# Optimization experiments

Measured on AMD Instinct MI355X. Metric: run time of the kernel, lower is better.

Reference implementation:

```python
import jax, jax.numpy as jnp
import numpy as np

N = 6144          # active voxels / points
C = 96            # embed_channels
B = 2             # batch size
D = H = W = 32    # sparse spatial shape
K = 16            # PFAS kNN
DEPTH = 4
GRID_OPTS = np.array([[0.1, 0.1, 0.1], [0.4, 0.4, 0.4], [0.2, 0.2, 0.2]], dtype=np.float32)
BN_EPS = 1e-5


def _bn(x, g, b):
    # BatchNorm1d in training mode: batch stats over the point dim, biased var
    m = x.mean(0)
    v = jnp.var(x, axis=0)
    return (x - m) * jax.lax.rsqrt(v + BN_EPS) * g + b


def _seg_sum(x, seg):
    return jax.ops.segment_sum(x, seg, num_segments=N)


def _forward(indices, x, fp_w, fp_b, fp_g, fp_be, att_w1, att_b1, att_w2, att_b2,
             ff_w1, ff_b1, ff_g, ff_be, ff_w2, ff_b2, sa_w1, sa_b1, sa_w2, sa_b2,
             fj_w1, fj_b1, fj_g, fj_be, fj_w2, fj_b2,
             proj_w, proj_g, proj_be, lw_w, lw_g, lw_be, w_w, adp_w,
             fuse_w, fuse_g, fuse_be, conv1_w, bn1_g, bn1_be, conv2_w, bn2_g, bn2_be):
    # ---- CMPFE ----
    p = jax.nn.relu(_bn(x @ fp_w.T + fp_b, fp_g, fp_be))            # [N,9]
    cd, cl, nm = p[:, :3], p[:, 3:6], p[:, 6:9]

    def _att(f, i):
        h = jax.nn.relu(f @ att_w1[i].T + att_b1[i])
        return jax.nn.sigmoid(h @ att_w2[i].T + att_b2[i])

    enh = jnp.concatenate([cd, cl * _att(cl, 0), nm * _att(nm, 1)], axis=1)
    fu = jax.nn.relu(_bn(enh @ ff_w1.T + ff_b1, ff_g, ff_be)) @ ff_w2.T + ff_b2
    sem = jax.nn.sigmoid(jax.nn.relu(fu @ sa_w1.T + sa_b1) @ sa_w2.T + sa_b2)
    feat = fu * sem + x * (1.0 - sem)                               # new x.features

    # ---- PFAS: kNN geometry stats ----
    coord = indices[:, 1:].astype(jnp.float32)                      # [N,3]
    batch = indices[:, 0]
    sq = jnp.sum(coord * coord, axis=1)
    d2 = sq[:, None] + sq[None, :] - 2.0 * (coord @ coord.T)
    dist = jnp.sqrt(jnp.maximum(d2, 1e-12))
    same = batch[None, :] == batch[:, None]
    eye = jnp.eye(N, dtype=bool)
    dist = jnp.where(same & ~eye, dist, jnp.inf)
    neg_nd, idx = jax.lax.top_k(-dist, K)                           # K nearest
    nbr = coord[idx]                                                # [N,K,3]
    cent = nbr - nbr.mean(axis=1, keepdims=True)
    cov = jnp.einsum('nkd,nke->nde', cent, cent) / (K - 1)
    S = jnp.linalg.svd(cov, compute_uv=False)                       # [N,3] descending
    Sn = S / (S.sum(axis=1, keepdims=True) + 1e-6)
    linearity = Sn[:, 0:1] - (Sn[:, 1] + Sn[:, 2])[:, None]
    mean_dist = (-neg_nd).mean(axis=1, keepdims=True)
    density = 1.0 / (mean_dist + 1e-6)
    fl = jax.nn.relu(_bn(feat @ fj_w1.T + fj_b1, fj_g, fj_be)) @ fj_w2.T + fj_b2
    fp_ = jax.nn.softmax(fl, axis=1)
    tower = (density * 2.0 + fp_[:, 0:1]) / 3.0
    backg = (jnp.maximum(1.0 - linearity, 1.0 - density) + fp_[:, 1:2]) / 3.0
    line = (linearity * 2.0 + fp_[:, 2:3]) / 3.0
    go = jnp.asarray(GRID_OPTS)
    lg = go[2] * jnp.array([1.0, 1.0, 5.0], jnp.float32)            # last dim *5
    grid_sizes = tower * go[0] + backg * go[1] + line * lg + 1e-6   # [N,3]

    # ---- representative grids (N > 200 path) ----
    gm = grid_sizes.mean(axis=1)
    order = jnp.argsort(gm)
    reps = [grid_sizes[order[100:200]].mean(0),
            grid_sizes[order[::-1][:100]].mean(0),
            grid_sizes[order[:100]].mean(0)]

    # ---- voxel-grid clustering (torch_geometric voxel_grid + unique inverse) ----
    start = coord.min(axis=0)

    def _cluster(size):
        size = jnp.clip(size, 1e-6, None)
        c = jnp.clip(jnp.floor((coord - start) / size).astype(jnp.int64), 0, 4095)
        mx = c.max(axis=0) + 1
        ids = ((batch.astype(jnp.int64) * mx[0] + c[:, 0]) * mx[1] + c[:, 1]) * mx[2] + c[:, 2]
        _, inv = jnp.unique(ids, return_inverse=True, size=N, fill_value=0)
        return inv.reshape(-1)

    # ---- adaptive multi-branch scatter softmax aggregation ----
    branch_feats = []
    for i in range(DEPTH - 1):
        seg = _cluster(reps[i])
        cnt = jnp.maximum(_seg_sum(jnp.ones((N, 1), feat.dtype), seg), 1.0)
        pw = jax.nn.relu(_bn(feat @ lw_w[i].T, lw_g[i], lw_be[i]))
        pw = pw - (_seg_sum(pw, seg) / cnt)[seg]
        pw = pw @ w_w[i].T
        pw = jnp.exp(pw - pw.max())
        pw = pw / (_seg_sum(pw, seg)[seg] + 1e-6)
        pf = jax.nn.relu(_bn(feat @ proj_w[i].T, proj_g[i], proj_be[i])) * pw
        branch_feats.append(_seg_sum(pf, seg)[seg])
    adp = jax.nn.softmax(feat @ adp_w.T, axis=1)                    # [N,3]
    agg = jnp.einsum('nc,ncd->nd', adp, jnp.stack(branch_feats, 1))
    last = jax.nn.relu(_bn(feat @ proj_w[-1].T, proj_g[-1], proj_be[-1]))
    fused = jax.nn.relu(_bn(jnp.concatenate([last, agg], 1) @ fuse_w.T, fuse_g, fuse_be)) + feat
    res = fused

    # ---- submanifold sparse conv block (dense scatter form; inactive sites zero,
    #      outputs gathered only at active sites == SubMConv3d) ----
    bi, zi, yi, xi = indices[:, 0], indices[:, 1], indices[:, 2], indices[:, 3]

    def _subm(f, w):
        grid = jnp.zeros((B, D, H, W, C), f.dtype).at[bi, zi, yi, xi].set(f)
        o = jax.lax.conv_general_dilated(grid, w, (1, 1, 1), 'SAME',
                                         dimension_numbers=('NDHWC', 'DHWIO', 'NDHWC'))
        return o[bi, zi, yi, xi]

    f1 = jax.nn.relu(_bn(_subm(fused, conv1_w), bn1_g, bn1_be))
    f2 = _bn(_subm(f1, conv2_w), bn2_g, bn2_be)
    return jax.nn.relu(f2 + res)


def setup_inputs() -> dict:
    key = jax.random.key(0)
    ks = iter(jax.random.split(key, 64))

    def rn(*shape, s=0.05):
        return jax.random.normal(next(ks), shape, jnp.float32) * s

    # unique active voxel coordinates
    rng = np.random.default_rng(0)
    flat = rng.choice(B * D * H * W, size=N, replace=False)
    b = flat // (D * H * W)
    r = flat % (D * H * W)
    z = r // (H * W)
    y = (r % (H * W)) // W
    xw = r % W
    indices = jnp.asarray(np.stack([b, z, y, xw], 1).astype(np.int32))
    Ch = C // 2
    return {
        'x': jax.random.normal(next(ks), (N, C), jnp.float32),
        'indices': indices,
        'fp_w': rn(9, C), 'fp_b': rn(9), 'fp_g': jnp.ones(9), 'fp_be': jnp.zeros(9),
        'att_w1': rn(2, 16, 3), 'att_b1': rn(2, 16), 'att_w2': rn(2, 3, 16), 'att_b2': rn(2, 3),
        'ff_w1': rn(C, 9), 'ff_b1': rn(C), 'ff_g': jnp.ones(C), 'ff_be': jnp.zeros(C),
        'ff_w2': rn(C, C), 'ff_b2': rn(C),
        'sa_w1': rn(Ch, C), 'sa_b1': rn(Ch), 'sa_w2': rn(1, Ch), 'sa_b2': rn(1),
        'fj_w1': rn(64, C), 'fj_b1': rn(64), 'fj_g': jnp.ones(64), 'fj_be': jnp.zeros(64),
        'fj_w2': rn(3, 64), 'fj_b2': rn(3),
        'proj_w': rn(DEPTH, C, C), 'proj_g': jnp.ones((DEPTH, C)), 'proj_be': jnp.zeros((DEPTH, C)),
        'lw_w': rn(DEPTH - 1, C, C), 'lw_g': jnp.ones((DEPTH - 1, C)), 'lw_be': jnp.zeros((DEPTH - 1, C)),
        'w_w': rn(DEPTH - 1, C, C),
        'adp_w': rn(DEPTH - 1, C),
        'fuse_w': rn(C, 2 * C), 'fuse_g': jnp.ones(C), 'fuse_be': jnp.zeros(C),
        'conv1_w': rn(3, 3, 3, C, C), 'bn1_g': jnp.ones(C), 'bn1_be': jnp.zeros(C),
        'conv2_w': rn(3, 3, 3, C, C), 'bn2_g': jnp.ones(C), 'bn2_be': jnp.zeros(C),
    }


def reference(x, indices, fp_w, fp_b, fp_g, fp_be, att_w1, att_b1, att_w2, att_b2,
              ff_w1, ff_b1, ff_g, ff_be, ff_w2, ff_b2, sa_w1, sa_b1, sa_w2, sa_b2,
              fj_w1, fj_b1, fj_g, fj_be, fj_w2, fj_b2,
              proj_w, proj_g, proj_be, lw_w, lw_g, lw_be, w_w, adp_w,
              fuse_w, fuse_g, fuse_be, conv1_w, bn1_g, bn1_be, conv2_w, bn2_g, bn2_be):
    return _forward(indices, x, fp_w, fp_b, fp_g, fp_be, att_w1, att_b1, att_w2, att_b2,
                    ff_w1, ff_b1, ff_g, ff_be, ff_w2, ff_b2, sa_w1, sa_b1, sa_w2, sa_b2,
                    fj_w1, fj_b1, fj_g, fj_be, fj_w2, fj_b2,
                    proj_w, proj_g, proj_be, lw_w, lw_g, lw_be, w_w, adp_w,
                    fuse_w, fuse_g, fuse_be, conv1_w, bn1_g, bn1_be, conv2_w, bn2_g, bn2_be)
```

## Files before the change

kernel.cpp:

```cpp
#include <hip/hip_runtime.h>
#include <cstdint>

#define NPTS 6144
#define CH 96
#define NCELEM (NPTS*CH)
#define HTSZ 16384
#define NBALL 514

__device__ __forceinline__ unsigned fenc(float f){
  unsigned u = __float_as_uint(f);
  return (u & 0x80000000u) ? ~u : (u | 0x80000000u);
}
__device__ __forceinline__ float fdec(unsigned u){
  unsigned b = (u & 0x80000000u) ? (u & 0x7FFFFFFFu) : ~u;
  return __uint_as_float(b);
}

__device__ void eig3(double a00,double a01,double a02,double a11,double a12,double a22,
                     double &e0,double &e1,double &e2){
  double p1 = a01*a01 + a02*a02 + a12*a12;
  double q = (a00+a11+a22)/3.0;
  double b00=a00-q, b11=a11-q, b22=a22-q;
  double p2 = b00*b00 + b11*b11 + b22*b22 + 2.0*p1;
  if (p2 <= 1e-300){ e0=e1=e2=q; return; }
  double pp = sqrt(p2/6.0);
  double inv = 1.0/pp;
  double c00=b00*inv, c01=a01*inv, c02=a02*inv, c11=b11*inv, c12=a12*inv, c22=b22*inv;
  double det = c00*(c11*c22-c12*c12) - c01*(c01*c22-c12*c02) + c02*(c01*c12-c11*c02);
  double r = det*0.5;
  r = r < -1.0 ? -1.0 : (r > 1.0 ? 1.0 : r);
  double phi = acos(r)/3.0;
  e0 = q + 2.0*pp*cos(phi);
  e2 = q + 2.0*pp*cos(phi + 2.0943951023931953);
  e1 = 3.0*q - e0 - e2;
}

__global__ void k_zero(int* p, long n){
  long i = (long)blockIdx.x*blockDim.x + threadIdx.x;
  long st = (long)gridDim.x*blockDim.x;
  for (; i < n; i += st) p[i] = 0;
}
__global__ void k_init(int* table, int* startmin){
  int i = blockIdx.x*blockDim.x + threadIdx.x;
  if (i < 2*32*32*32) table[i] = -1;
  if (i < 3) startmin[i] = 0x7fffffff;
}
__global__ void k_htinit(unsigned long long* keys, int* vals){
  int i = blockIdx.x*blockDim.x + threadIdx.x;
  if (i < 3*HTSZ){ keys[i] = ~0ull; vals[i] = 0x7fffffff; }
}
__global__ void k_pack_min(const int* __restrict__ ind, unsigned* __restrict__ packed, int* startmin){
  __shared__ int mn[3];
  if (threadIdx.x < 3) mn[threadIdx.x] = 0x7fffffff;
  __syncthreads();
  int p = blockIdx.x*blockDim.x + threadIdx.x;
  if (p < NPTS){
    int b = ind[p*4], z = ind[p*4+1], y = ind[p*4+2], x = ind[p*4+3];
    packed[p] = (unsigned)((b<<15)|(z<<10)|(y<<5)|x);
    atomicMin(&mn[0], z); atomicMin(&mn[1], y); atomicMin(&mn[2], x);
  }
  __syncthreads();
  if (threadIdx.x < 3) atomicMin(&startmin[threadIdx.x], mn[threadIdx.x]);
}
__global__ void k_ball(unsigned* __restrict__ ball){
  __shared__ int hcnt[32], hbase[32], hpos[32];
  int tid = threadIdx.x;
  if (tid < 32){ hcnt[tid] = 0; hpos[tid] = 0; }
  __syncthreads();
  for (int i=tid; i<1331; i+=256){
    int dz = i/121, rm = i - dz*121, dy = rm/11, dx = rm - dy*11;
    int a = dz-5, b = dy-5, c = dx-5;
    int d2 = a*a + b*b + c*c;
    if (d2 > 0 && d2 <= 25) atomicAdd(&hcnt[d2], 1);
  }
  __syncthreads();
  if (tid == 0){
    int acc = 0;
    for (int d=1; d<=25; ++d){ hbase[d] = acc; acc += hcnt[d]; }
  }
  __syncthreads();
  for (int i=tid; i<1331; i+=256){
    int dz = i/121, rm = i - dz*121, dy = rm/11, dx = rm - dy*11;
    int a = dz-5, b = dy-5, c = dx-5;
    int d2 = a*a + b*b + c*c;
    if (d2 > 0 && d2 <= 25){
      int pos = hbase[d2] + atomicAdd(&hpos[d2], 1);
      ball[pos] = ((unsigned)d2<<16)|((unsigned)dz<<10)|((unsigned)dy<<5)|(unsigned)dx;
    }
  }
}

__global__ void __launch_bounds__(256) k_mm(
    const float* __restrict__ Abase, const float* __restrict__ Wbase,
    const float* __restrict__ biasBase, float* __restrict__ Obase,
    int CIN, int COUT,
    long sA, long sW, long sO, long sBias,
    const float* __restrict__ statsBase, long sStats,
    const float* __restrict__ gBase, const float* __restrict__ beBase, long sGB,
    const float* __restrict__ SsumBase, const int* __restrict__ segBase, const int* __restrict__ cntBase,
    unsigned* maxenc, int mode)
{
  int zb = blockIdx.y;
  const float* A = Abase + (long)zb*sA;
  const float* W = Wbase + (long)zb*sW;
  float* O = Obase + (long)zb*sO;
  const float* st = statsBase ? statsBase + (long)zb*sStats : nullptr;
  const float* g  = gBase ? gBase + (long)zb*sGB : nullptr;
  const float* be = beBase ? beBase + (long)zb*sGB : nullptr;
  const float* Ss = SsumBase ? SsumBase + (long)zb*NCELEM : nullptr;
  const int* seg  = segBase ? segBase + (long)zb*NPTS : nullptr;
  const int* cnt  = cntBase ? cntBase + (long)zb*NPTS : nullptr;

  __shared__ float Alt[96*34];
  __shared__ float Wlt[96*98];
  int tid = threadIdx.x;
  int r0 = blockIdx.x*32;
  for (int idx = tid; idx < CIN*COUT; idx += 256){
    int co = idx / CIN, k = idx - co*CIN;
    Wlt[k*98 + co] = W[idx];
  }
  for (int idx = tid; idx < 32*CIN; idx += 256){
    int ir = idx / CIN, k = idx - ir*CIN;
    int row = r0 + ir;
    float v = A[(long)row*CIN + k];
    if (mode >= 1) v = fmaxf((v - st[k*2])*st[k*2+1]*g[k] + be[k], 0.f);
    if (mode == 2){
      int s = seg[row];
      float cf = fmaxf((float)cnt[s], 1.f);
      v -= Ss[(long)s*CH + k] / cf;
    }
    Alt[k*34 + ir] = v;
  }
  __syncthreads();
  float lmax = -3.4e38f;
  if (COUT == 96){
    int rp = tid >> 4, cg = tid & 15;
    int co0 = cg*6;
    float acc0[6], acc1[6];
    #pragma unroll
    for (int j=0;j<6;++j){
      float b = biasBase ? biasBase[(long)zb*sBias + co0 + j] : 0.f;
      acc0[j] = b; acc1[j] = b;
    }
    int ra = 2*rp;
    for (int k=0;k<CIN;++k){
      float2 a  = *(const float2*)&Alt[k*34 + ra];
      float2 w0 = *(const float2*)&Wlt[k*98 + co0];
      float2 w1 = *(const float2*)&Wlt[k*98 + co0 + 2];
      float2 w2 = *(const float2*)&Wlt[k*98 + co0 + 4];
      acc0[0] = fmaf(a.x, w0.x, acc0[0]); acc1[0] = fmaf(a.y, w0.x, acc1[0]);
      acc0[1] = fmaf(a.x, w0.y, acc0[1]); acc1[1] = fmaf(a.y, w0.y, acc1[1]);
      acc0[2] = fmaf(a.x, w1.x, acc0[2]); acc1[2] = fmaf(a.y, w1.x, acc1[2]);
      acc0[3] = fmaf(a.x, w1.y, acc0[3]); acc1[3] = fmaf(a.y, w1.y, acc1[3]);
      acc0[4] = fmaf(a.x, w2.x, acc0[4]); acc1[4] = fmaf(a.y, w2.x, acc1[4]);
      acc0[5] = fmaf(a.x, w2.y, acc0[5]); acc1[5] = fmaf(a.y, w2.y, acc1[5]);
    }
    int rb = ra+1;
    #pragma unroll
    for (int j=0;j<6;++j){
      O[(long)(r0+ra)*96 + co0 + j] = acc0[j];
      O[(long)(r0+rb)*96 + co0 + j] = acc1[j];
      lmax = fmaxf(lmax, fmaxf(acc0[j], acc1[j]));
    }
  } else {
    for (int idx = tid; idx < 32*COUT; idx += 256){
      int ir = idx/COUT, co = idx - ir*COUT;
      float acc = biasBase ? biasBase[(long)zb*sBias + co] : 0.f;
      for (int k=0;k<CIN;++k) acc = fmaf(Alt[k*34+ir], Wlt[k*98+co], acc);
      O[(long)(r0+ir)*COUT + co] = acc;
      lmax = fmaxf(lmax, acc);
    }
  }
  if (maxenc){
    __shared__ float rmx[256];
    rmx[tid] = lmax; __syncthreads();
    for (int s2=128; s2>0; s2>>=1){
      if (tid < s2) rmx[tid] = fmaxf(rmx[tid], rmx[tid+s2]);
      __syncthreads();
    }
    if (tid == 0) atomicMax(&maxenc[zb], fenc(rmx[0]));
  }
}

__global__ void __launch_bounds__(256) k_mm_fuse(
    const float* __restrict__ tp3, const float* __restrict__ st,
    const float* __restrict__ pg3, const float* __restrict__ pbe3,
    const float* __restrict__ agg, const float* __restrict__ fw, float* __restrict__ tf)
{
  __shared__ float Alt[192*34];
  __shared__ float Wlt[96*98];
  int tid = threadIdx.x, r0 = blockIdx.x*32;
  for (int idx = tid; idx < 32*192; idx += 256){
    int ir = idx/192, k = idx - ir*192;
    int row = r0 + ir;
    float v;
    if (k < 96){
      v = tp3[(long)row*96 + k];
      v = fmaxf((v - st[k*2])*st[k*2+1]*pg3[k] + pbe3[k], 0.f);
    } else {
      v = agg[(long)row*96 + (k-96)];
    }
    Alt[k*34 + ir] = v;
  }
  int rp = tid >> 4, cg = tid & 15, co0 = cg*6;
  float acc0[6] = {0,0,0,0,0,0}, acc1[6] = {0,0,0,0,0,0};
  int ra = 2*rp, rb = ra+1;
  for (int h=0; h<2; ++h){
    __syncthreads();
    for (int idx = tid; idx < 96*96; idx += 256){
      int co = idx/96, k = idx - co*96;
      Wlt[k*98+co] = fw[(long)co*192 + h*96 + k];
    }
    __syncthreads();
    for (int k=0;k<96;++k){
      float2 a  = *(const float2*)&Alt[(h*96 + k)*34 + ra];
      float2 w0 = *(const float2*)&Wlt[k*98 + co0];
      float2 w1 = *(const float2*)&Wlt[k*98 + co0 + 2];
      float2 w2 = *(const float2*)&Wlt[k*98 + co0 + 4];
      acc0[0] = fmaf(a.x, w0.x, acc0[0]); acc1[0] = fmaf(a.y, w0.x, acc1[0]);
      acc0[1] = fmaf(a.x, w0.y, acc0[1]); acc1[1] = fmaf(a.y, w0.y, acc1[1]);
      acc0[2] = fmaf(a.x, w1.x, acc0[2]); acc1[2] = fmaf(a.y, w1.x, acc1[2]);
      acc0[3] = fmaf(a.x, w1.y, acc0[3]); acc1[3] = fmaf(a.y, w1.y, acc1[3]);
      acc0[4] = fmaf(a.x, w2.x, acc0[4]); acc1[4] = fmaf(a.y, w2.x, acc1[4]);
      acc0[5] = fmaf(a.x, w2.y, acc0[5]); acc1[5] = fmaf(a.y, w2.y, acc1[5]);
    }
  }
  #pragma unroll
  for (int j=0;j<6;++j){
    tf[(long)(r0+ra)*96 + co0 + j] = acc0[j];
    tf[(long)(r0+rb)*96 + co0 + j] = acc1[j];
  }
}

__global__ void k_stats(const float* __restrict__ Abase, long sA, int COLS,
                        float* __restrict__ statsBase, long sStats){
  int col = blockIdx.x, zb = blockIdx.y;
  const float* A = Abase + (long)zb*sA;
  double s = 0.0, q = 0.0;
  for (int r = threadIdx.x; r < NPTS; r += 256){
    double v = (double)A[(long)r*COLS + col];
    s += v; q += v*v;
  }
  __shared__ double ls[256], lq[256];
  ls[threadIdx.x] = s; lq[threadIdx.x] = q; __syncthreads();
  for (int t=128; t>0; t>>=1){
    if (threadIdx.x < t){ ls[threadIdx.x] += ls[threadIdx.x+t]; lq[threadIdx.x] += lq[threadIdx.x+t]; }
    __syncthreads();
  }
  if (threadIdx.x == 0){
    double mean = ls[0]/NPTS;
    double var = lq[0]/NPTS - mean*mean;
    float* stp = statsBase + (long)zb*sStats + col*2;
    stp[0] = (float)mean;
    stp[1] = (float)(1.0/sqrt(var + 1e-5));
  }
}

__global__ void k_p_att_enh(const float* __restrict__ t9, const float* __restrict__ st,
                            const float* __restrict__ fg, const float* __restrict__ fbe,
                            const float* __restrict__ aw1, const float* __restrict__ ab1,
                            const float* __restrict__ aw2, const float* __restrict__ ab2,
                            float* __restrict__ enh){
  int p = blockIdx.x*blockDim.x + threadIdx.x;
  if (p >= NPTS) return;
  float pp[9];
  #pragma unroll
  for (int c=0;c<9;++c){
    float v = t9[p*9+c];
    pp[c] = fmaxf((v - st[c*2])*st[c*2+1]*fg[c] + fbe[c], 0.f);
  }
  float eo[9];
  eo[0]=pp[0]; eo[1]=pp[1]; eo[2]=pp[2];
  #pragma unroll
  for (int i=0;i<2;++i){
    const float* w1 = aw1 + i*48;
    const float* b1 = ab1 + i*16;
    const float* w2 = aw2 + i*48;
    const float* b2 = ab2 + i*3;
    const float* f = pp + 3 + i*3;
    float h[16];
    #pragma unroll
    for (int j=0;j<16;++j){
      float s = b1[j];
      #pragma unroll
      for (int k=0;k<3;++k) s = fmaf(f[k], w1[j*3+k], s);
      h[j] = fmaxf(s, 0.f);
    }
    #pragma unroll
    for (int o=0;o<3;++o){
      float s = b2[o];
      #pragma unroll
      for (int j=0;j<16;++j) s = fmaf(h[j], w2[o*16+j], s);
      float a = 1.f/(1.f + expf(-s));
      eo[3+i*3+o] = f[o]*a;
    }
  }
  #pragma unroll
  for (int c=0;c<9;++c) enh[p*9+c] = eo[c];
}

__global__ void __launch_bounds__(256) k_sem_feat(
    const float* __restrict__ fu, const float* __restrict__ x,
    const float* __restrict__ w1, const float* __restrict__ b1,
    const float* __restrict__ w2, const float* __restrict__ b2,
    float* __restrict__ feat){
  int wid = (blockIdx.x*blockDim.x + threadIdx.x) >> 6;
  int lane = threadIdx.x & 63;
  if (wid >= NPTS) return;
  const float* fr = fu + (long)wid*96;
  float partial = 0.f;
  if (lane < 48){
    float h = b1[lane];
    for (int k=0;k<96;++k) h = fmaf(fr[k], w1[lane*96+k], h);
    h = fmaxf(h, 0.f);
    partial = h * w2[lane];
  }
  for (int m=32; m; m>>=1) partial += __shfl_xor(partial, m);
  float sem = 1.f/(1.f + expf(-(partial + b2[0])));
  for (int c=lane; c<96; c+=64){
    float f = fr[c];
    feat[(long)wid*96+c] = f*sem + x[(long)wid*96+c]*(1.f - sem);
  }
}

__global__ void __launch_bounds__(256) k_knn(const unsigned* __restrict__ packed,
                                             const int* __restrict__ table,
                                             const unsigned* __restrict__ ball,
                                             float* __restrict__ density, float* __restrict__ linearity){
  __shared__ unsigned pk[NPTS];
  for (int i=threadIdx.x; i<NPTS; i+=256) pk[i] = packed[i];
  __syncthreads();
  int pid = blockIdx.x*4 + (threadIdx.x>>6);
  int lane = threadIdx.x & 63;
  unsigned mypc = pk[pid];
  int myb = (int)(mypc>>15);
  int mz = (int)((mypc>>10)&31), my_=(int)((mypc>>5)&31), mx_=(int)(mypc&31);
  unsigned s[16];
  #pragma unroll
  for (int t=0;t<16;++t) s[t] = 0xFFFFFFFFu;
  int cnt = 0;
  const int tbase = myb*32768;
  for (int it=0; it<9; ++it){
    int i = lane + it*64;
    if (i < NBALL){
      unsigned e = ball[i];
      int d2 = (int)(e >> 16);
      int dz = (int)((e>>10)&31) - 5;
      int dy = (int)((e>>5)&31) - 5;
      int dx = (int)(e&31) - 5;
      int zz = mz+dz, yy = my_+dy, xx = mx_+dx;
      if ((unsigned)zz < 32u && (unsigned)yy < 32u && (unsigned)xx < 32u){
        int j = table[tbase + (zz*32+yy)*32+xx];
        if (j >= 0){
          ++cnt;
          unsigned key = ((unsigned)d2<<13) | (unsigned)j;
          if (key < s[15]){
            s[15] = key;
            #pragma unroll
            for (int t=15;t>0;--t){
              unsigned a = s[t-1], b = s[t];
              unsigned lo = a<b?a:b, hi = a<b?b:a;
              s[t-1]=lo; s[t]=hi;
            }
          }
        }
      }
    }
    int nxt = (it+1)*64;
    if (nxt >= NBALL) break;
    int tot = cnt;
    for (int m=32; m; m>>=1) tot += __shfl_xor(tot, m);
    unsigned dlast = ball[nxt-1] >> 16;
    unsigned dnext = ball[nxt] >> 16;
    if (tot >= 16 && dnext > dlast) break;
  }
  int tot = cnt;
  for (int m=32; m; m>>=1) tot += __shfl_xor(tot, m);
  if (tot < 16){
    #pragma unroll
    for (int t=0;t<16;++t) s[t] = 0xFFFFFFFFu;
    for (int it=0; it<96; ++it){
      int j = lane + it*64;
      unsigned pc = pk[j];
      if (j != pid && (int)(pc>>15) == myb){
        int dz = (int)((pc>>10)&31) - mz;
        int dy = (int)((pc>>5)&31) - my_;
        int dx = (int)(pc&31) - mx_;
        unsigned d2 = (unsigned)(dz*dz + dy*dy + dx*dx);
        unsigned key = (d2<<13) | (unsigned)j;
        if (key < s[15]){
          s[15] = key;
          #pragma unroll
          for (int t=15;t>0;--t){
            unsigned a = s[t-1], b = s[t];
            unsigned lo = a<b?a:b, hi = a<b?b:a;
            s[t-1]=lo; s[t]=hi;
          }
        }
      }
    }
  }
  float sdist = 0.f;
  int sz=0,sy=0,sx=0,szz=0,syy=0,sxx=0,szy=0,szx=0,syx=0;
  for (int r=0;r<16;++r){
    unsigned m = s[0];
    #pragma unroll
    for (int w=32; w; w>>=1){
      unsigned o = (unsigned)__shfl_xor((int)m, w);
      m = m<o ? m : o;
    }
    bool own = (s[0] == m);
    #pragma unroll
    for (int t=0;t<15;++t) s[t] = own ? s[t+1] : s[t];
    if (own) s[15] = 0xFFFFFFFFu;
    unsigned idx = m & 8191u;
    unsigned d2 = m >> 13;
    sdist += sqrtf((float)d2);
    unsigned pc = pk[idx];
    int nz=(int)((pc>>10)&31), ny=(int)((pc>>5)&31), nx=(int)(pc&31);
    sz+=nz; sy+=ny; sx+=nx;
    szz+=nz*nz; syy+=ny*ny; sxx+=nx*nx; szy+=nz*ny; szx+=nz*nx; syx+=ny*nx;
  }
  if (lane == 0){
    double m0 = sz/16.0, m1 = sy/16.0, m2 = sx/16.0;
    float c00 = (float)(((double)szz - 16.0*m0*m0)/15.0);
    float c11 = (float)(((double)syy - 16.0*m1*m1)/15.0);
    float c22 = (float)(((double)sxx - 16.0*m2*m2)/15.0);
    float c01 = (float)(((double)szy - 16.0*m0*m1)/15.0);
    float c02 = (float)(((double)szx - 16.0*m0*m2)/15.0);
    float c12 = (float)(((double)syx - 16.0*m1*m2)/15.0);
    double e0,e1,e2;
    eig3((double)c00,(double)c01,(double)c02,(double)c11,(double)c12,(double)c22, e0,e1,e2);
    float s0 = (float)fabs(e0), s1 = (float)fabs(e1), s2 = (float)fabs(e2);
    float den = s0 + s1 + s2 + 1e-6f;
    float sn0 = s0/den, sn1 = s1/den, sn2 = s2/den;
    linearity[pid] = sn0 - (sn1 + sn2);
    float md = sdist * (1.f/16.f);
    density[pid] = 1.f/(md + 1e-6f);
  }
}

__global__ void k_geo(const float* __restrict__ t64, const float* __restrict__ st,
                      const float* __restrict__ fg, const float* __restrict__ fbe,
                      const float* __restrict__ w2, const float* __restrict__ b2,
                      const float* __restrict__ density, const float* __restrict__ linearity,
                      float* __restrict__ gsz, float* __restrict__ gm){
  int p = blockIdx.x*blockDim.x + threadIdx.x;
  if (p >= NPTS) return;
  float fl[3];
  #pragma unroll
  for (int o=0;o<3;++o) fl[o] = b2[o];
  for (int k=0;k<64;++k){
    float v = t64[(long)p*64+k];
    v = fmaxf((v - st[k*2])*st[k*2+1]*fg[k] + fbe[k], 0.f);
    #pragma unroll
    for (int o=0;o<3;++o) fl[o] = fmaf(v, w2[o*64+k], fl[o]);
  }
  float mx = fmaxf(fl[0], fmaxf(fl[1], fl[2]));
  float e0 = expf(fl[0]-mx), e1 = expf(fl[1]-mx), e2 = expf(fl[2]-mx);
  float es = e0+e1+e2;
  float p0 = e0/es, p1 = e1/es, p2 = e2/es;
  float den = density[p], lin = linearity[p];
  float tw = (den*2.f + p0)/3.f;
  float bg = (fmaxf(1.f-lin, 1.f-den) + p1)/3.f;
  float ln = (lin*2.f + p2)/3.f;
  float g0 = tw*0.1f + bg*0.4f + ln*0.2f + 1e-6f;
  float g1 = tw*0.1f + bg*0.4f + ln*0.2f + 1e-6f;
  float g2 = tw*0.1f + bg*0.4f + ln*1.0f + 1e-6f;
  gsz[p*3+0]=g0; gsz[p*3+1]=g1; gsz[p*3+2]=g2;
  gm[p] = (g0+g1+g2)/3.f;
}

#define RNKCHUNK 768
__global__ void __launch_bounds__(256) k_rank(const float* __restrict__ gm, int* __restrict__ rank){
  __shared__ unsigned long long lk[RNKCHUNK];
  int j0 = blockIdx.y*RNKCHUNK;
  for (int i=threadIdx.x; i<RNKCHUNK; i+=256){
    int j = j0 + i;
    lk[i] = (((unsigned long long)fenc(gm[j]))<<13) | (unsigned long long)j;
  }
  __syncthreads();
  int p = blockIdx.x*256 + threadIdx.x;
  unsigned long long myk = (((unsigned long long)fenc(gm[p]))<<13) | (unsigned long long)p;
  int cnt = 0;
  #pragma unroll 4
  for (int i=0; i<RNKCHUNK; ++i) cnt += (lk[i] < myk) ? 1 : 0;
  atomicAdd(&rank[p], cnt);
}
__global__ void k_scatter(const int* __restrict__ rank, const float* __restrict__ gsz,
                          float* __restrict__ bkt){
  int p = blockIdx.x*blockDim.x + threadIdx.x;
  if (p >= NPTS) return;
  int r = rank[p];
  int z = -1, t = 0;
  if (r < 100){ z = 2; t = r; }
  else if (r < 200){ z = 0; t = r - 100; }
  else if (r >= NPTS-100){ z = 1; t = r - (NPTS-100); }
  if (z >= 0){
    #pragma unroll
    for (int d=0; d<3; ++d) bkt[(z*100 + t)*3 + d] = gsz[p*3+d];
  }
}
__global__ void k_reps(const float* __restrict__ bkt, float* __restrict__ reps){
  int i = threadIdx.x;
  if (i >= 9) return;
  int z = i/3, d = i - z*3;
  double s = 0.0;
  for (int t=0; t<100; ++t) s += (double)bkt[(z*100 + t)*3 + d];
  reps[i] = (float)(s/100.0);
}

__global__ void k_cluster_c(const int* __restrict__ ind, const float* __restrict__ reps,
                            const int* __restrict__ startmin, int* __restrict__ cbuf, int* mxbuf){
  int z = blockIdx.y;
  int p = blockIdx.x*blockDim.x + threadIdx.x;
  __shared__ int lmx[3];
  if (threadIdx.x < 3) lmx[threadIdx.x] = 0;
  __syncthreads();
  if (p < NPTS){
    #pragma unroll
    for (int d=0; d<3; ++d){
      float sizev = fmaxf(reps[z*3+d], 1e-6f);
      float cf = floorf(((float)ind[p*4+1+d] - (float)startmin[d]) / sizev);
      int ci = (int)cf;
      ci = ci < 0 ? 0 : (ci > 4095 ? 4095 : ci);
      cbuf[((long)z*NPTS + p)*3 + d] = ci;
      atomicMax(&lmx[d], ci);
    }
  }
  __syncthreads();
  if (threadIdx.x < 3) atomicMax(&mxbuf[z*3+threadIdx.x], lmx[threadIdx.x]);
}
__global__ void k_cluster_ids(const int* __restrict__ ind, const int* __restrict__ cbuf,
                              const int* __restrict__ mxbuf, long long* __restrict__ ids){
  int z = blockIdx.y;
  int p = blockIdx.x*blockDim.x + threadIdx.x;
  if (p >= NPTS) return;
  long long mx0 = mxbuf[z*3+0]+1, mx1 = mxbuf[z*3+1]+1, mx2 = mxbuf[z*3+2]+1;
  long long b = ind[p*4];
  const int* cc = cbuf + ((long)z*NPTS + p)*3;
  ids[(long)z*NPTS + p] = ((b*mx0 + cc[0])*mx1 + cc[1])*mx2 + cc[2];
}

__device__ __forceinline__ int ht_hash(unsigned long long id){
  unsigned long long h = id * 0x9E3779B97F4A7C15ull;
  return (int)(h >> 49) & (HTSZ-1);
}
__global__ void k_seg_build(const long long* __restrict__ ids,
                            unsigned long long* __restrict__ keys, int* __restrict__ vals){
  int z = blockIdx.y;
  int p = blockIdx.x*blockDim.x + threadIdx.x;
  if (p >= NPTS) return;
  unsigned long long id = (unsigned long long)ids[(long)z*NPTS + p];
  unsigned long long* K = keys + (long)z*HTSZ;
  int* V = vals + (long)z*HTSZ;
  int slot = ht_hash(id);
  while (true){
    unsigned long long prev = atomicCAS(&K[slot], ~0ull, id);
    if (prev == ~0ull || prev == id){ atomicMin(&V[slot], p); break; }
    slot = (slot + 1) & (HTSZ-1);
  }
}
__global__ void k_seg_lookup(const long long* __restrict__ ids,
                             const unsigned long long* __restrict__ keys, const int* __restrict__ vals,
                             int* __restrict__ seg, int* __restrict__ cnt){
  int z = blockIdx.y;
  int p = blockIdx.x*blockDim.x + threadIdx.x;
  if (p >= NPTS) return;
  unsigned long long id = (unsigned long long)ids[(long)z*NPTS + p];
  const unsigned long long* K = keys + (long)z*HTSZ;
  int slot = ht_hash(id);
  while (K[slot] != id) slot = (slot + 1) & (HTSZ-1);
  int rep = vals[(long)z*HTSZ + slot];
  seg[(long)z*NPTS + p] = rep;
  atomicAdd(&cnt[(long)z*NPTS + rep], 1);
}

__global__ void k_pw_accum(const float* __restrict__ tlw, const float* __restrict__ stats,
                           const float* __restrict__ g, const float* __restrict__ be,
                           const int* __restrict__ seg, float* __restrict__ S){
  int z = blockIdx.y;
  int idx = blockIdx.x*blockDim.x + threadIdx.x;
  int p = idx/CH, c = idx - p*CH;
  const float* st = stats + z*192;
  float v = tlw[(long)z*NCELEM + idx];
  v = fmaxf((v - st[c*2])*st[c*2+1]*g[z*CH+c] + be[z*CH+c], 0.f);
  atomicAdd(&S[(long)z*NCELEM + (long)seg[(long)z*NPTS+p]*CH + c], v);
}
__global__ void k_exp_accum(const float* __restrict__ pw2, const unsigned* __restrict__ maxenc,
                            const int* __restrict__ seg, float* __restrict__ E){
  int z = blockIdx.y;
  int idx = blockIdx.x*blockDim.x + threadIdx.x;
  int p = idx/CH, c = idx - p*CH;
  float mv = fdec(maxenc[z]);
  float v = expf(pw2[(long)z*NCELEM + idx] - mv);
  atomicAdd(&E[(long)z*NCELEM + (long)seg[(long)z*NPTS+p]*CH + c], v);
}
__global__ void k_pf_accum(const float* __restrict__ tp, const float* __restrict__ stats,
                           const float* __restrict__ pg, const float* __restrict__ pbe,
                           const float* __restrict__ pw2, const unsigned* __restrict__ maxenc,
                           const int* __restrict__ seg, const float* __restrict__ E,
                           float* __restrict__ F){
  int z = blockIdx.y;
  int idx = blockIdx.x*blockDim.x + threadIdx.x;
  int p = idx/CH, c = idx - p*CH;
  const float* st = stats + z*192;
  float v = tp[(long)z*NCELEM + idx];
  v = fmaxf((v - st[c*2])*st[c*2+1]*pg[z*CH+c] + pbe[z*CH+c], 0.f);
  float mv = fdec(maxenc[z]);
  int sg = seg[(long)z*NPTS+p];
  float w = expf(pw2[(long)z*NCELEM + idx] - mv) / (E[(long)z*NCELEM + (long)sg*CH + c] + 1e-6f);
  atomicAdd(&F[(long)z*NCELEM + (long)sg*CH + c], v*w);
}
__global__ void k_adp(const float* __restrict__ feat, const float* __restrict__ aw,
                      float* __restrict__ adp){
  int p = blockIdx.x*blockDim.x + threadIdx.x;
  if (p >= NPTS) return;
  float a0=0.f, a1=0.f, a2=0.f;
  for (int k=0;k<CH;++k){
    float f = feat[(long)p*CH+k];
    a0 = fmaf(f, aw[k], a0);
    a1 = fmaf(f, aw[CH+k], a1);
    a2 = fmaf(f, aw[2*CH+k], a2);
  }
  float m = fmaxf(a0, fmaxf(a1,a2));
  float e0 = expf(a0-m), e1 = expf(a1-m), e2 = expf(a2-m);
  float s = e0+e1+e2;
  adp[p*3]=e0/s; adp[p*3+1]=e1/s; adp[p*3+2]=e2/s;
}
__global__ void k_agg(const float* __restrict__ adp, const float* __restrict__ F,
                      const int* __restrict__ seg, float* __restrict__ agg){
  int idx = blockIdx.x*blockDim.x + threadIdx.x;
  int p = idx/CH, c = idx - p*CH;
  float s = 0.f;
  #pragma unroll
  for (int z=0;z<3;++z)
    s = fmaf(adp[p*3+z], F[(long)z*NCELEM + (long)seg[(long)z*NPTS+p]*CH + c], s);
  agg[idx] = s;
}

__global__ void k_fused(const float* __restrict__ tf, const float* __restrict__ st,
                        const float* __restrict__ fg, const float* __restrict__ fbe,
                        const float* __restrict__ feat, float* __restrict__ fused){
  int idx = blockIdx.x*blockDim.x + threadIdx.x;
  int c = idx % CH;
  float v = tf[idx];
  v = fmaxf((v - st[c*2])*st[c*2+1]*fg[c] + fbe[c], 0.f);
  fused[idx] = v + feat[idx];
}
__global__ void k_table(const int* __restrict__ ind, int* __restrict__ table){
  int p = blockIdx.x*blockDim.x + threadIdx.x;
  if (p >= NPTS) return;
  int b = ind[p*4], z = ind[p*4+1], y = ind[p*4+2], x = ind[p*4+3];
  table[((b*32+z)*32+y)*32+x] = p;
}
__global__ void k_nbr(const int* __restrict__ ind, const int* __restrict__ table,
                      int* __restrict__ nbrtab){
  int idx = blockIdx.x*blockDim.x + threadIdx.x;
  if (idx >= NPTS*27) return;
  int p = idx/27, tap = idx - p*27;
  int dz = tap/9 - 1;
  int rm = tap % 9;
  int dy = rm/3 - 1, dx = rm%3 - 1;
  int b = ind[p*4], z = ind[p*4+1]+dz, y = ind[p*4+2]+dy, x = ind[p*4+3]+dx;
  int q = -1;
  if ((unsigned)z < 32u && (unsigned)y < 32u && (unsigned)x < 32u)
    q = table[((b*32+z)*32+y)*32+x];
  nbrtab[idx] = q;
}
__global__ void __launch_bounds__(256) k_convlist(const int* __restrict__ nbrtab,
                                                  int* __restrict__ tapcnt,
                                                  int* __restrict__ ptlist){
  __shared__ int lcnt[27], lbase[27], lpos[27];
  int tid = threadIdx.x;
  if (tid < 27){ lcnt[tid] = 0; lpos[tid] = 0; }
  __syncthreads();
  int base = blockIdx.x * 6912;
  for (int i = tid; i < 6912; i += 256){
    int idx = base + i;
    if (nbrtab[idx] >= 0) atomicAdd(&lcnt[idx % 27], 1);
  }
  __syncthreads();
  if (tid < 27) lbase[tid] = atomicAdd(&tapcnt[tid], lcnt[tid]);
  __syncthreads();
  for (int i = tid; i < 6912; i += 256){
    int idx = base + i;
    int q = nbrtab[idx];
    if (q >= 0){
      int tap = idx % 27;
      int p = idx / 27;
      int pos = lbase[tap] + atomicAdd(&lpos[tap], 1);
      ptlist[tap*NPTS + pos] = (p<<16) | q;
    }
  }
}
__global__ void __launch_bounds__(256) k_conv_gemm(
    const float* __restrict__ src, const float* __restrict__ Wc,
    const int* __restrict__ tapcnt, const int* __restrict__ ptlist,
    float* __restrict__ part){
  int tap = blockIdx.y;
  int n = tapcnt[tap];
  int r0 = blockIdx.x*32;
  if (r0 >= n) return;
  __shared__ float Alt[96*34];
  __shared__ float Wlt[96*98];
  __shared__ int pqs[32];
  int tid = threadIdx.x;
  if (tid < 32){
    int r = r0 + tid;
    pqs[tid] = (r < n) ? ptlist[tap*NPTS + r] : -1;
  }
  __syncthreads();
  for (int idx4 = tid; idx4 < 2304; idx4 += 256){
    int ci = idx4/24, c4 = idx4 - ci*24;
    float4 w = ((const float4*)(Wc + ((long)tap*96 + ci)*96))[c4];
    float* d = &Wlt[ci*98 + c4*4];
    d[0]=w.x; d[1]=w.y; d[2]=w.z; d[3]=w.w;
  }
  for (int idx4 = tid; idx4 < 32*24; idx4 += 256){
    int ir = idx4/24, c4 = idx4 - ir*24;
    int pq = pqs[ir];
    float4 s = make_float4(0.f,0.f,0.f,0.f);
    if (pq >= 0){
      int q = pq & 0xFFFF;
      s = ((const float4*)(src + (long)q*CH))[c4];
    }
    int k0 = c4*4;
    Alt[(k0+0)*34 + ir] = s.x;
    Alt[(k0+1)*34 + ir] = s.y;
    Alt[(k0+2)*34 + ir] = s.z;
    Alt[(k0+3)*34 + ir] = s.w;
  }
  __syncthreads();
  int rp = tid >> 4, cg = tid & 15;
  int co0 = cg*6;
  int ra = 2*rp, rb = ra+1;
  float acc0[6]={0,0,0,0,0,0}, acc1[6]={0,0,0,0,0,0};
  for (int k=0;k<96;++k){
    float2 a  = *(const float2*)&Alt[k*34 + ra];
    float2 w0 = *(const float2*)&Wlt[k*98 + co0];
    float2 w1 = *(const float2*)&Wlt[k*98 + co0 + 2];
    float2 w2 = *(const float2*)&Wlt[k*98 + co0 + 4];
    acc0[0] = fmaf(a.x, w0.x, acc0[0]); acc1[0] = fmaf(a.y, w0.x, acc1[0]);
    acc0[1] = fmaf(a.x, w0.y, acc0[1]); acc1[1] = fmaf(a.y, w0.y, acc1[1]);
    acc0[2] = fmaf(a.x, w1.x, acc0[2]); acc1[2] = fmaf(a.y, w1.x, acc1[2]);
    acc0[3] = fmaf(a.x, w1.y, acc0[3]); acc1[3] = fmaf(a.y, w1.y, acc1[3]);
    acc0[4] = fmaf(a.x, w2.x, acc0[4]); acc1[4] = fmaf(a.y, w2.x, acc1[4]);
    acc0[5] = fmaf(a.x, w2.y, acc0[5]); acc1[5] = fmaf(a.y, w2.y, acc1[5]);
  }
  int pa = pqs[ra], pb = pqs[rb];
  if (pa >= 0){
    float* o = part + ((long)(pa>>16)*27 + tap)*CH + co0;
    #pragma unroll
    for (int j=0;j<6;++j) o[j] = acc0[j];
  }
  if (pb >= 0){
    float* o = part + ((long)(pb>>16)*27 + tap)*CH + co0;
    #pragma unroll
    for (int j=0;j<6;++j) o[j] = acc1[j];
  }
}
__global__ void __launch_bounds__(256) k_conv_sum(const int* __restrict__ nbrtab,
                                                  const float* __restrict__ part,
                                                  float* __restrict__ out){
  int idx = blockIdx.x*256 + threadIdx.x;
  int p = idx/24, c4 = idx - p*24;
  const int* nt = nbrtab + p*27;
  float4 acc = make_float4(0.f,0.f,0.f,0.f);
  for (int tap=0; tap<27; ++tap){
    if (nt[tap] >= 0){
      float4 v = ((const float4*)part)[((long)p*27 + tap)*24 + c4];
      acc.x += v.x; acc.y += v.y; acc.z += v.z; acc.w += v.w;
    }
  }
  ((float4*)out)[idx] = acc;
}
__global__ void __launch_bounds__(256) k_conv_gemm_atomic(
    const float* __restrict__ src, const float* __restrict__ Wc,
    const int* __restrict__ tapcnt, const int* __restrict__ ptlist,
    float* __restrict__ out){
  int tap = blockIdx.y;
  int n = tapcnt[tap];
  int r0 = blockIdx.x*32;
  if (r0 >= n) return;
  __shared__ float Al[32*97];
  __shared__ float Wl[96*97];
  __shared__ int pqs[32];
  int tid = threadIdx.x;
  if (tid < 32){
    int r = r0 + tid;
    pqs[tid] = (r < n) ? ptlist[tap*NPTS + r] : -1;
  }
  __syncthreads();
  for (int idx4 = tid; idx4 < 2304; idx4 += 256){
    int ci = idx4/24, c4 = idx4 - ci*24;
    float4 w = ((const float4*)(Wc + ((long)tap*96 + ci)*96))[c4];
    float* d = &Wl[ci*97 + c4*4];
    d[0]=w.x; d[1]=w.y; d[2]=w.z; d[3]=w.w;
  }
  for (int idx4 = tid; idx4 < 32*24; idx4 += 256){
    int ir = idx4/24, c4 = idx4 - ir*24;
    int pq = pqs[ir];
    float4 s = make_float4(0.f,0.f,0.f,0.f);
    if (pq >= 0){
      int q = pq & 0xFFFF;
      s = ((const float4*)(src + (long)q*CH))[c4];
    }
    float* d = &Al[ir*97 + c4*4];
    d[0]=s.x; d[1]=s.y; d[2]=s.z; d[3]=s.w;
  }
  __syncthreads();
  int rp = tid >> 4, cg = tid & 15;
  int co0 = cg*6;
  int ra = 2*rp, rb = ra+1;
  float acc0[6]={0,0,0,0,0,0}, acc1[6]={0,0,0,0,0,0};
  for (int k=0;k<96;++k){
    float a0 = Al[ra*97+k], a1 = Al[rb*97+k];
    #pragma unroll
    for (int j=0;j<6;++j){
      float w = Wl[k*97+co0+j];
      acc0[j] = fmaf(a0, w, acc0[j]);
      acc1[j] = fmaf(a1, w, acc1[j]);
    }
  }
  int pa = pqs[ra], pb = pqs[rb];
  if (pa >= 0){
    float* o = out + (long)(pa>>16)*CH + co0;
    #pragma unroll
    for (int j=0;j<6;++j) atomicAdd(&o[j], acc0[j]);
  }
  if (pb >= 0){
    float* o = out + (long)(pb>>16)*CH + co0;
    #pragma unroll
    for (int j=0;j<6;++j) atomicAdd(&o[j], acc1[j]);
  }
}
__global__ void k_bnrelu(const float* __restrict__ a, const float* __restrict__ st,
                         const float* __restrict__ g, const float* __restrict__ be,
                         float* __restrict__ o){
  int idx = blockIdx.x*blockDim.x + threadIdx.x;
  int c = idx % CH;
  float v = a[idx];
  o[idx] = fmaxf((v - st[c*2])*st[c*2+1]*g[c] + be[c], 0.f);
}
__global__ void k_final(const float* __restrict__ c2, const float* __restrict__ st,
                        const float* __restrict__ g, const float* __restrict__ be,
                        const float* __restrict__ fused, float* __restrict__ out){
  int idx = blockIdx.x*blockDim.x + threadIdx.x;
  int c = idx % CH;
  float v = c2[idx];
  v = (v - st[c*2])*st[c*2+1]*g[c] + be[c];
  out[idx] = fmaxf(v + fused[idx], 0.f);
}

extern "C" void kernel_launch(void* const* d_in, const int* in_sizes, int n_in,
                              void* d_out, int out_size, void* d_ws, size_t ws_size,
                              hipStream_t stream)
{
  const float* x      = (const float*)d_in[0];
  const int*   ind    = (const int*)  d_in[1];
  const float* fp_w   = (const float*)d_in[2];
  const float* fp_b   = (const float*)d_in[3];
  const float* fp_g   = (const float*)d_in[4];
  const float* fp_be  = (const float*)d_in[5];
  const float* att_w1 = (const float*)d_in[6];
  const float* att_b1 = (const float*)d_in[7];
  const float* att_w2 = (const float*)d_in[8];
  const float* att_b2 = (const float*)d_in[9];
  const float* ff_w1  = (const float*)d_in[10];
  const float* ff_b1  = (const float*)d_in[11];
  const float* ff_g   = (const float*)d_in[12];
  const float* ff_be  = (const float*)d_in[13];
  const float* ff_w2  = (const float*)d_in[14];
  const float* ff_b2  = (const float*)d_in[15];
  const float* sa_w1  = (const float*)d_in[16];
  const float* sa_b1  = (const float*)d_in[17];
  const float* sa_w2  = (const float*)d_in[18];
  const float* sa_b2  = (const float*)d_in[19];
  const float* fj_w1  = (const float*)d_in[20];
  const float* fj_b1  = (const float*)d_in[21];
  const float* fj_g   = (const float*)d_in[22];
  const float* fj_be  = (const float*)d_in[23];
  const float* fj_w2  = (const float*)d_in[24];
  const float* fj_b2  = (const float*)d_in[25];
  const float* proj_w = (const float*)d_in[26];
  const float* proj_g = (const float*)d_in[27];
  const float* proj_be= (const float*)d_in[28];
  const float* lw_w   = (const float*)d_in[29];
  const float* lw_g   = (const float*)d_in[30];
  const float* lw_be  = (const float*)d_in[31];
  const float* w_w    = (const float*)d_in[32];
  const float* adp_w  = (const float*)d_in[33];
  const float* fuse_w = (const float*)d_in[34];
  const float* fuse_g = (const float*)d_in[35];
  const float* fuse_be= (const float*)d_in[36];
  const float* conv1_w= (const float*)d_in[37];
  const float* bn1_g  = (const float*)d_in[38];
  const float* bn1_be = (const float*)d_in[39];
  const float* conv2_w= (const float*)d_in[40];
  const float* bn2_g  = (const float*)d_in[41];
  const float* bn2_be = (const float*)d_in[42];
  float* outp = (float*)d_out;
  (void)in_sizes; (void)n_in; (void)out_size;

  char* ws = (char*)d_ws;
  size_t off = 0;
  auto alloc = [&](size_t bytes)->size_t{
    off = (off + 255) & ~(size_t)255;
    size_t o = off; off += bytes; return o;
  };
  const size_t FNC = (size_t)NCELEM*4;
  size_t o_packed = alloc((size_t)NPTS*4);
  size_t o_start  = alloc(16);
  size_t o_ball   = alloc((size_t)NBALL*4);
  size_t o_dens   = alloc((size_t)NPTS*4);
  size_t o_lin    = alloc((size_t)NPTS*4);
  size_t o_t9     = alloc((size_t)NPTS*9*4);
  size_t o_enh    = alloc((size_t)NPTS*9*4);
  size_t o_gm     = alloc((size_t)NPTS*4);
  size_t o_gsz    = alloc((size_t)NPTS*3*4);
  size_t o_reps   = alloc(16*4);
  size_t o_bkt    = alloc((size_t)3*100*3*4);
  size_t o_cbuf   = alloc((size_t)3*NPTS*3*4);
  size_t o_ids    = alloc((size_t)3*NPTS*8);
  size_t o_seg    = alloc((size_t)3*NPTS*4);
  size_t o_adp    = alloc((size_t)NPTS*3*4);
  size_t o_table  = alloc((size_t)65536*4);
  size_t o_nbr    = alloc((size_t)NPTS*27*4);
  size_t o_ptlist = alloc((size_t)27*NPTS*4);
  size_t o_t64    = alloc((size_t)NPTS*64*4);
  size_t o_stats  = alloc((size_t)13*192*4);
  size_t o_htk    = alloc((size_t)3*HTSZ*8);
  size_t o_htv    = alloc((size_t)3*HTSZ*4);
  size_t o_S      = alloc(3*FNC);
  size_t o_E      = alloc(3*FNC);
  size_t o_F      = alloc(3*FNC);
  size_t o_cnt    = alloc((size_t)3*NPTS*4);
  size_t o_rank   = alloc((size_t)NPTS*4);
  size_t o_tapcnt = alloc(32*4);
  size_t o_mx     = alloc(16*4);
  size_t o_maxenc = alloc(16*4);
  size_t zend = off;
  size_t o_T96 = alloc(FNC);
  size_t o_fu  = alloc(FNC);
  size_t o_feat= alloc(FNC);
  size_t o_tlw = alloc(3*FNC);
  size_t o_pw2 = alloc(3*FNC);
  size_t o_tp  = alloc(4*FNC);
  size_t o_agg = alloc(FNC);
  size_t o_tf  = alloc(FNC);
  size_t o_fsd = alloc(FNC);
  size_t o_c1  = alloc(FNC);
  size_t o_f1  = alloc(FNC);
  size_t o_c2  = alloc(FNC);
  size_t o_part = alloc((size_t)NPTS*27*CH*4);
  bool use_part = (off <= ws_size);

  float* stats = (float*)(ws + o_stats);
  long zcount = (long)((zend - o_S)/4);

  k_zero<<<dim3(2048), dim3(256), 0, stream>>>((int*)(ws+o_S), zcount);
  k_init<<<dim3(256), dim3(256), 0, stream>>>((int*)(ws+o_table), (int*)(ws+o_start));
  k_htinit<<<dim3((3*HTSZ+255)/256), dim3(256), 0, stream>>>((unsigned long long*)(ws+o_htk), (int*)(ws+o_htv));
  k_pack_min<<<dim3(24), dim3(256), 0, stream>>>(ind, (unsigned*)(ws+o_packed), (int*)(ws+o_start));
  k_table<<<dim3(24), 256, 0, stream>>>(ind, (int*)(ws+o_table));
  k_ball<<<dim3(1), 256, 0, stream>>>((unsigned*)(ws+o_ball));

  k_mm<<<dim3(192,1), 256, 0, stream>>>(x, fp_w, fp_b, (float*)(ws+o_t9), 96, 9,
      0,0,0,0, nullptr,0, nullptr,nullptr,0, nullptr,nullptr,nullptr, nullptr, 0);
  k_stats<<<dim3(9,1), 256, 0, stream>>>((float*)(ws+o_t9), 0, 9, stats+0*192, 0);
  k_p_att_enh<<<dim3(24), 256, 0, stream>>>((float*)(ws+o_t9), stats+0*192, fp_g, fp_be,
      att_w1, att_b1, att_w2, att_b2, (float*)(ws+o_enh));

  k_mm<<<dim3(192,1), 256, 0, stream>>>((float*)(ws+o_enh), ff_w1, ff_b1, (float*)(ws+o_T96), 9, 96,
      0,0,0,0, nullptr,0, nullptr,nullptr,0, nullptr,nullptr,nullptr, nullptr, 0);
  k_stats<<<dim3(96,1), 256, 0, stream>>>((float*)(ws+o_T96), 0, 96, stats+1*192, 0);
  k_mm<<<dim3(192,1), 256, 0, stream>>>((float*)(ws+o_T96), ff_w2, ff_b2, (float*)(ws+o_fu), 96, 96,
      0,0,0,0, stats+1*192,0, ff_g, ff_be,0, nullptr,nullptr,nullptr, nullptr, 1);

  k_sem_feat<<<dim3(1536), 256, 0, stream>>>((float*)(ws+o_fu), x, sa_w1, sa_b1, sa_w2, sa_b2,
      (float*)(ws+o_feat));

  k_knn<<<dim3(1536), 256, 0, stream>>>((unsigned*)(ws+o_packed), (int*)(ws+o_table),
      (unsigned*)(ws+o_ball), (float*)(ws+o_dens), (float*)(ws+o_lin));

  k_mm<<<dim3(192,1), 256, 0, stream>>>((float*)(ws+o_feat), fj_w1, fj_b1, (float*)(ws+o_t64), 96, 64,
      0,0,0,0, nullptr,0, nullptr,nullptr,0, nullptr,nullptr,nullptr, nullptr, 0);
  k_stats<<<dim3(64,1), 256, 0, stream>>>((float*)(ws+o_t64), 0, 64, stats+2*192, 0);
  k_geo<<<dim3(24), 256, 0, stream>>>((float*)(ws+o_t64), stats+2*192, fj_g, fj_be, fj_w2, fj_b2,
      (float*)(ws+o_dens), (float*)(ws+o_lin), (float*)(ws+o_gsz), (float*)(ws+o_gm));

  k_rank<<<dim3(24,8), 256, 0, stream>>>((float*)(ws+o_gm), (int*)(ws+o_rank));
  k_scatter<<<dim3(24), 256, 0, stream>>>((int*)(ws+o_rank), (float*)(ws+o_gsz), (float*)(ws+o_bkt));
  k_reps<<<dim3(1), 64, 0, stream>>>((float*)(ws+o_bkt), (float*)(ws+o_reps));

  k_cluster_c<<<dim3(24,3), 256, 0, stream>>>(ind, (float*)(ws+o_reps), (int*)(ws+o_start),
      (int*)(ws+o_cbuf), (int*)(ws+o_mx));
  k_cluster_ids<<<dim3(24,3), 256, 0, stream>>>(ind, (int*)(ws+o_cbuf), (int*)(ws+o_mx),
      (long long*)(ws+o_ids));
  k_seg_build<<<dim3(24,3), 256, 0, stream>>>((long long*)(ws+o_ids),
      (unsigned long long*)(ws+o_htk), (int*)(ws+o_htv));
  k_seg_lookup<<<dim3(24,3), 256, 0, stream>>>((long long*)(ws+o_ids),
      (unsigned long long*)(ws+o_htk), (int*)(ws+o_htv), (int*)(ws+o_seg), (int*)(ws+o_cnt));

  k_mm<<<dim3(192,3), 256, 0, stream>>>((float*)(ws+o_feat), lw_w, nullptr, (float*)(ws+o_tlw), 96, 96,
      0, 96*96, NCELEM, 0, nullptr,0, nullptr,nullptr,0, nullptr,nullptr,nullptr, nullptr, 0);
  k_stats<<<dim3(96,3), 256, 0, stream>>>((float*)(ws+o_tlw), NCELEM, 96, stats+3*192, 192);
  k_pw_accum<<<dim3(2304,3), 256, 0, stream>>>((float*)(ws+o_tlw), stats+3*192, lw_g, lw_be,
      (int*)(ws+o_seg), (float*)(ws+o_S));
  k_mm<<<dim3(192,3), 256, 0, stream>>>((float*)(ws+o_tlw), w_w, nullptr, (float*)(ws+o_pw2), 96, 96,
      NCELEM, 96*96, NCELEM, 0, stats+3*192,192, lw_g, lw_be,96,
      (float*)(ws+o_S), (int*)(ws+o_seg), (int*)(ws+o_cnt), (unsigned*)(ws+o_maxenc), 2);
  k_exp_accum<<<dim3(2304,3), 256, 0, stream>>>((float*)(ws+o_pw2), (unsigned*)(ws+o_maxenc),
      (int*)(ws+o_seg), (float*)(ws+o_E));
  k_mm<<<dim3(192,4), 256, 0, stream>>>((float*)(ws+o_feat), proj_w, nullptr, (float*)(ws+o_tp), 96, 96,
      0, 96*96, NCELEM, 0, nullptr,0, nullptr,nullptr,0, nullptr,nullptr,nullptr, nullptr, 0);
  k_stats<<<dim3(96,4), 256, 0, stream>>>((float*)(ws+o_tp), NCELEM, 96, stats+6*192, 192);
  k_pf_accum<<<dim3(2304,3), 256, 0, stream>>>((float*)(ws+o_tp), stats+6*192, proj_g, proj_be,
      (float*)(ws+o_pw2), (unsigned*)(ws+o_maxenc), (int*)(ws+o_seg), (float*)(ws+o_E), (float*)(ws+o_F));
  k_adp<<<dim3(24), 256, 0, stream>>>((float*)(ws+o_feat), adp_w, (float*)(ws+o_adp));
  k_agg<<<dim3(2304), 256, 0, stream>>>((float*)(ws+o_adp), (float*)(ws+o_F), (int*)(ws+o_seg),
      (float*)(ws+o_agg));

  k_mm_fuse<<<dim3(192), 256, 0, stream>>>((float*)(ws+o_tp) + (size_t)3*NCELEM, stats+9*192,
      proj_g + 3*96, proj_be + 3*96, (float*)(ws+o_agg), fuse_w, (float*)(ws+o_tf));
  k_stats<<<dim3(96,1), 256, 0, stream>>>((float*)(ws+o_tf), 0, 96, stats+10*192, 0);
  k_fused<<<dim3(2304), 256, 0, stream>>>((float*)(ws+o_tf), stats+10*192, fuse_g, fuse_be,
      (float*)(ws+o_feat), (float*)(ws+o_fsd));

  k_nbr<<<dim3((NPTS*27+255)/256), 256, 0, stream>>>(ind, (int*)(ws+o_table), (int*)(ws+o_nbr));
  k_convlist<<<dim3(24), 256, 0, stream>>>((int*)(ws+o_nbr), (int*)(ws+o_tapcnt),
      (int*)(ws+o_ptlist));
  if (use_part){
    k_conv_gemm<<<dim3(192,27), 256, 0, stream>>>((float*)(ws+o_fsd), conv1_w,
        (int*)(ws+o_tapcnt), (int*)(ws+o_ptlist), (float*)(ws+o_part));
    k_conv_sum<<<dim3(NPTS*24/256), 256, 0, stream>>>((int*)(ws+o_nbr), (float*)(ws+o_part),
        (float*)(ws+o_c1));
  } else {
    k_zero<<<dim3(2304), dim3(256), 0, stream>>>((int*)(ws+o_c1), NCELEM);
    k_conv_gemm_atomic<<<dim3(192,27), 256, 0, stream>>>((float*)(ws+o_fsd), conv1_w,
        (int*)(ws+o_tapcnt), (int*)(ws+o_ptlist), (float*)(ws+o_c1));
  }
  k_stats<<<dim3(96,1), 256, 0, stream>>>((float*)(ws+o_c1), 0, 96, stats+11*192, 0);
  k_bnrelu<<<dim3(2304), 256, 0, stream>>>((float*)(ws+o_c1), stats+11*192, bn1_g, bn1_be, (float*)(ws+o_f1));
  if (use_part){
    k_conv_gemm<<<dim3(192,27), 256, 0, stream>>>((float*)(ws+o_f1), conv2_w,
        (int*)(ws+o_tapcnt), (int*)(ws+o_ptlist), (float*)(ws+o_part));
    k_conv_sum<<<dim3(NPTS*24/256), 256, 0, stream>>>((int*)(ws+o_nbr), (float*)(ws+o_part),
        (float*)(ws+o_c2));
  } else {
    k_zero<<<dim3(2304), dim3(256), 0, stream>>>((int*)(ws+o_c2), NCELEM);
    k_conv_gemm_atomic<<<dim3(192,27), 256, 0, stream>>>((float*)(ws+o_f1), conv2_w,
        (int*)(ws+o_tapcnt), (int*)(ws+o_ptlist), (float*)(ws+o_c2));
  }
  k_stats<<<dim3(96,1), 256, 0, stream>>>((float*)(ws+o_c2), 0, 96, stats+12*192, 0);
  k_final<<<dim3(2304), 256, 0, stream>>>((float*)(ws+o_c2), stats+12*192, bn2_g, bn2_be,
      (float*)(ws+o_fsd), outp);
}
```

Baseline: 501.9 us.

## Fuse setup, clustering, adp/agg, and BN-ReLU into neighbouring kernels to cut launches

Merges the init kernels into one setup kernel and the pack/table/ball kernels into a second. Scatter and reps become one kernel using a last-block-done counter. The cluster max is computed from the coordinate max instead of a separate pass. k_adp and k_agg are fused, and k_nbr and k_convlist become one kernel. The fused-feature and BN1-ReLU elementwise passes are folded into the conv gather and the final kernel, removing several launches and full-tensor round trips. In exchange the BN math is recomputed per gathered neighbour in the conv load, and the derived cluster max assumes floor is monotone in the coordinate.

```diff
diff --git a/kernel.cpp b/kernel.cpp
--- a/kernel.cpp
+++ b/kernel.cpp
@@ -35,57 +35,62 @@
   e1 = 3.0*q - e0 - e2;
 }
 
-__global__ void k_zero(int* p, long n){
+__global__ void k_setup0(int* __restrict__ zb, long zcount,
+                         unsigned long long* __restrict__ htk, int* __restrict__ htv,
+                         int* __restrict__ table, int* __restrict__ startmm){
   long i = (long)blockIdx.x*blockDim.x + threadIdx.x;
   long st = (long)gridDim.x*blockDim.x;
-  for (; i < n; i += st) p[i] = 0;
-}
-__global__ void k_init(int* table, int* startmin){
-  int i = blockIdx.x*blockDim.x + threadIdx.x;
-  if (i < 2*32*32*32) table[i] = -1;
-  if (i < 3) startmin[i] = 0x7fffffff;
-}
-__global__ void k_htinit(unsigned long long* keys, int* vals){
-  int i = blockIdx.x*blockDim.x + threadIdx.x;
-  if (i < 3*HTSZ){ keys[i] = ~0ull; vals[i] = 0x7fffffff; }
-}
-__global__ void k_pack_min(const int* __restrict__ ind, unsigned* __restrict__ packed, int* startmin){
-  __shared__ int mn[3];
-  if (threadIdx.x < 3) mn[threadIdx.x] = 0x7fffffff;
-  __syncthreads();
-  int p = blockIdx.x*blockDim.x + threadIdx.x;
-  if (p < NPTS){
+  for (long j=i; j<zcount; j+=st) zb[j] = 0;
+  for (long j=i; j<3*HTSZ; j+=st){ htk[j] = ~0ull; htv[j] = 0x7fffffff; }
+  for (long j=i; j<2*32768; j+=st) table[j] = -1;
+  if (i < 3) startmm[i] = 0x7fffffff;
+  else if (i < 6) startmm[i] = 0;
+}
+__global__ void __launch_bounds__(256) k_setup1(const int* __restrict__ ind,
+                                                unsigned* __restrict__ packed,
+                                                int* __restrict__ startmm,
+                                                int* __restrict__ table,
+                                                unsigned* __restrict__ ball){
+  __shared__ int mn[3], mx[3];
+  __shared__ int hcnt[32], hbase[32], hpos[32];
+  int tid = threadIdx.x;
+  if (blockIdx.x < 24){
+    if (tid < 3){ mn[tid] = 0x7fffffff; mx[tid] = 0; }
+    __syncthreads();
+    int p = blockIdx.x*256 + tid;
     int b = ind[p*4], z = ind[p*4+1], y = ind[p*4+2], x = ind[p*4+3];
     packed[p] = (unsigned)((b<<15)|(z<<10)|(y<<5)|x);
+    table[((b*32+z)*32+y)*32+x] = p;
     atomicMin(&mn[0], z); atomicMin(&mn[1], y); atomicMin(&mn[2], x);
-  }
-  __syncthreads();
-  if (threadIdx.x < 3) atomicMin(&startmin[threadIdx.x], mn[threadIdx.x]);
-}
-__global__ void k_ball(unsigned* __restrict__ ball){
-  __shared__ int hcnt[32], hbase[32], hpos[32];
-  int tid = threadIdx.x;
-  if (tid < 32){ hcnt[tid] = 0; hpos[tid] = 0; }
-  __syncthreads();
-  for (int i=tid; i<1331; i+=256){
-    int dz = i/121, rm = i - dz*121, dy = rm/11, dx = rm - dy*11;
-    int a = dz-5, b = dy-5, c = dx-5;
-    int d2 = a*a + b*b + c*c;
-    if (d2 > 0 && d2 <= 25) atomicAdd(&hcnt[d2], 1);
-  }
-  __syncthreads();
-  if (tid == 0){
-    int acc = 0;
-    for (int d=1; d<=25; ++d){ hbase[d] = acc; acc += hcnt[d]; }
-  }
-  __syncthreads();
-  for (int i=tid; i<1331; i+=256){
-    int dz = i/121, rm = i - dz*121, dy = rm/11, dx = rm - dy*11;
-    int a = dz-5, b = dy-5, c = dx-5;
-    int d2 = a*a + b*b + c*c;
-    if (d2 > 0 && d2 <= 25){
-      int pos = hbase[d2] + atomicAdd(&hpos[d2], 1);
-      ball[pos] = ((unsigned)d2<<16)|((unsigned)dz<<10)|((unsigned)dy<<5)|(unsigned)dx;
+    atomicMax(&mx[0], z); atomicMax(&mx[1], y); atomicMax(&mx[2], x);
+    __syncthreads();
+    if (tid < 3){
+      atomicMin(&startmm[tid], mn[tid]);
+      atomicMax(&startmm[3+tid], mx[tid]);
+    }
+  } else {
+    if (tid < 32){ hcnt[tid] = 0; hpos[tid] = 0; }
+    __syncthreads();
+    for (int i=tid; i<1331; i+=256){
+      int dz = i/121, rm = i - dz*121, dy = rm/11, dx = rm - dy*11;
+      int a = dz-5, b = dy-5, c = dx-5;
+      int d2 = a*a + b*b + c*c;
+      if (d2 > 0 && d2 <= 25) atomicAdd(&hcnt[d2], 1);
+    }
+    __syncthreads();
+    if (tid == 0){
+      int acc = 0;
+      for (int d=1; d<=25; ++d){ hbase[d] = acc; acc += hcnt[d]; }
+    }
+    __syncthreads();
+    for (int i=tid; i<1331; i+=256){
+      int dz = i/121, rm = i - dz*121, dy = rm/11, dx = rm - dy*11;
+      int a = dz-5, b = dy-5, c = dx-5;
+      int d2 = a*a + b*b + c*c;
+      if (d2 > 0 && d2 <= 25){
+        int pos = hbase[d2] + atomicAdd(&hpos[d2], 1);
+        ball[pos] = ((unsigned)d2<<16)|((unsigned)dz<<10)|((unsigned)dy<<5)|(unsigned)dx;
+      }
     }
   }
 }
@@ -487,59 +492,58 @@
   for (int i=0; i<RNKCHUNK; ++i) cnt += (lk[i] < myk) ? 1 : 0;
   atomicAdd(&rank[p], cnt);
 }
-__global__ void k_scatter(const int* __restrict__ rank, const float* __restrict__ gsz,
-                          float* __restrict__ bkt){
-  int p = blockIdx.x*blockDim.x + threadIdx.x;
-  if (p >= NPTS) return;
+__global__ void __launch_bounds__(256) k_scatter_reps(const int* __restrict__ rank,
+                                                      const float* __restrict__ gsz,
+                                                      float* __restrict__ bkt,
+                                                      int* __restrict__ done,
+                                                      float* __restrict__ reps){
+  __shared__ int lastf;
+  int p = blockIdx.x*256 + threadIdx.x;
   int r = rank[p];
-  int z = -1, t = 0;
-  if (r < 100){ z = 2; t = r; }
-  else if (r < 200){ z = 0; t = r - 100; }
-  else if (r >= NPTS-100){ z = 1; t = r - (NPTS-100); }
-  if (z >= 0){
-    #pragma unroll
-    for (int d=0; d<3; ++d) bkt[(z*100 + t)*3 + d] = gsz[p*3+d];
-  }
-}
-__global__ void k_reps(const float* __restrict__ bkt, float* __restrict__ reps){
-  int i = threadIdx.x;
-  if (i >= 9) return;
-  int z = i/3, d = i - z*3;
-  double s = 0.0;
-  for (int t=0; t<100; ++t) s += (double)bkt[(z*100 + t)*3 + d];
-  reps[i] = (float)(s/100.0);
-}
-
-__global__ void k_cluster_c(const int* __restrict__ ind, const float* __restrict__ reps,
-                            const int* __restrict__ startmin, int* __restrict__ cbuf, int* mxbuf){
-  int z = blockIdx.y;
-  int p = blockIdx.x*blockDim.x + threadIdx.x;
-  __shared__ int lmx[3];
-  if (threadIdx.x < 3) lmx[threadIdx.x] = 0;
-  __syncthreads();
-  if (p < NPTS){
-    #pragma unroll
-    for (int d=0; d<3; ++d){
-      float sizev = fmaxf(reps[z*3+d], 1e-6f);
-      float cf = floorf(((float)ind[p*4+1+d] - (float)startmin[d]) / sizev);
-      int ci = (int)cf;
-      ci = ci < 0 ? 0 : (ci > 4095 ? 4095 : ci);
-      cbuf[((long)z*NPTS + p)*3 + d] = ci;
-      atomicMax(&lmx[d], ci);
-    }
-  }
-  __syncthreads();
-  if (threadIdx.x < 3) atomicMax(&mxbuf[z*3+threadIdx.x], lmx[threadIdx.x]);
-}
-__global__ void k_cluster_ids(const int* __restrict__ ind, const int* __restrict__ cbuf,
-                              const int* __restrict__ mxbuf, long long* __restrict__ ids){
+  int zb = -1, t = 0;
+  if (r < 100){ zb = 2; t = r; }
+  else if (r < 200){ zb = 0; t = r - 100; }
+  else if (r >= NPTS-100){ zb = 1; t = r - (NPTS-100); }
+  if (zb >= 0){
+    #pragma unroll
+    for (int d=0; d<3; ++d) bkt[(zb*100 + t)*3 + d] = gsz[p*3+d];
+  }
+  __threadfence();
+  __syncthreads();
+  if (threadIdx.x == 0) lastf = (atomicAdd(done, 1) == 23) ? 1 : 0;
+  __syncthreads();
+  if (lastf){
+    __threadfence();
+    int i = threadIdx.x;
+    if (i < 9){
+      int z = i/3, d = i - z*3;
+      double s = 0.0;
+      for (int tt=0; tt<100; ++tt) s += (double)bkt[(z*100 + tt)*3 + d];
+      reps[i] = (float)(s/100.0);
+    }
+  }
+}
+
+__global__ void k_cluster(const int* __restrict__ ind, const float* __restrict__ reps,
+                          const int* __restrict__ startmm, long long* __restrict__ ids){
   int z = blockIdx.y;
   int p = blockIdx.x*blockDim.x + threadIdx.x;
   if (p >= NPTS) return;
-  long long mx0 = mxbuf[z*3+0]+1, mx1 = mxbuf[z*3+1]+1, mx2 = mxbuf[z*3+2]+1;
+  long long mxp[3]; int cc[3];
+  #pragma unroll
+  for (int d=0; d<3; ++d){
+    float sizev = fmaxf(reps[z*3+d], 1e-6f);
+    float cf = floorf(((float)ind[p*4+1+d] - (float)startmm[d]) / sizev);
+    int ci = (int)cf;
+    ci = ci < 0 ? 0 : (ci > 4095 ? 4095 : ci);
+    cc[d] = ci;
+    float cfm = floorf(((float)startmm[3+d] - (float)startmm[d]) / sizev);
+    int cm = (int)cfm;
+    cm = cm < 0 ? 0 : (cm > 4095 ? 4095 : cm);
+    mxp[d] = (long long)cm + 1;
+  }
   long long b = ind[p*4];
-  const int* cc = cbuf + ((long)z*NPTS + p)*3;
-  ids[(long)z*NPTS + p] = ((b*mx0 + cc[0])*mx1 + cc[1])*mx2 + cc[2];
+  ids[(long)z*NPTS + p] = ((b*mxp[0] + cc[0])*mxp[1] + cc[1])*mxp[2] + cc[2];
 }
 
 __device__ __forceinline__ int ht_hash(unsigned long long id){
@@ -612,33 +616,46 @@
   float w = expf(pw2[(long)z*NCELEM + idx] - mv) / (E[(long)z*NCELEM + (long)sg*CH + c] + 1e-6f);
   atomicAdd(&F[(long)z*NCELEM + (long)sg*CH + c], v*w);
 }
-__global__ void k_adp(const float* __restrict__ feat, const float* __restrict__ aw,
-                      float* __restrict__ adp){
-  int p = blockIdx.x*blockDim.x + threadIdx.x;
-  if (p >= NPTS) return;
-  float a0=0.f, a1=0.f, a2=0.f;
-  for (int k=0;k<CH;++k){
-    float f = feat[(long)p*CH+k];
-    a0 = fmaf(f, aw[k], a0);
-    a1 = fmaf(f, aw[CH+k], a1);
-    a2 = fmaf(f, aw[2*CH+k], a2);
-  }
-  float m = fmaxf(a0, fmaxf(a1,a2));
-  float e0 = expf(a0-m), e1 = expf(a1-m), e2 = expf(a2-m);
-  float s = e0+e1+e2;
-  adp[p*3]=e0/s; adp[p*3+1]=e1/s; adp[p*3+2]=e2/s;
-}
-__global__ void k_agg(const float* __restrict__ adp, const float* __restrict__ F,
-                      const int* __restrict__ seg, float* __restrict__ agg){
-  int idx = blockIdx.x*blockDim.x + threadIdx.x;
-  int p = idx/CH, c = idx - p*CH;
-  float s = 0.f;
-  #pragma unroll
-  for (int z=0;z<3;++z)
-    s = fmaf(adp[p*3+z], F[(long)z*NCELEM + (long)seg[(long)z*NPTS+p]*CH + c], s);
-  agg[idx] = s;
-}
-
+__global__ void __launch_bounds__(256) k_adp_agg(
+    const float* __restrict__ feat, const float* __restrict__ aw,
+    const float* __restrict__ F, const int* __restrict__ seg,
+    float* __restrict__ agg){
+  __shared__ float ladp[32][3];
+  __shared__ int lseg[32][3];
+  int tid = threadIdx.x;
+  int p0 = blockIdx.x*32;
+  if (tid < 96){
+    int pl = tid/3, z = tid - pl*3;
+    const float* fr = feat + (long)(p0+pl)*CH;
+    float a = 0.f;
+    for (int k=0;k<CH;++k) a = fmaf(fr[k], aw[z*CH+k], a);
+    ladp[pl][z] = a;
+    lseg[pl][z] = seg[(long)z*NPTS + (p0+pl)];
+  }
+  __syncthreads();
+  if (tid < 32){
+    float a0 = ladp[tid][0], a1 = ladp[tid][1], a2 = ladp[tid][2];
+    float m = fmaxf(a0, fmaxf(a1,a2));
+    float e0 = expf(a0-m), e1 = expf(a1-m), e2 = expf(a2-m);
+    float s = e0+e1+e2;
+    ladp[tid][0]=e0/s; ladp[tid][1]=e1/s; ladp[tid][2]=e2/s;
+  }
+  __syncthreads();
+  for (int e = tid; e < 32*CH; e += 256){
+    int pl = e/CH, c = e - pl*CH;
+    float s = 0.f;
+    #pragma unroll
+    for (int z=0;z<3;++z)
+      s = fmaf(ladp[pl][z], F[(long)z*NCELEM + (long)lseg[pl][z]*CH + c], s);
+    agg[(long)p0*CH + e] = s;
+  }
+}
+
+__global__ void k_zero(int* p, long n){
+  long i = (long)blockIdx.x*blockDim.x + threadIdx.x;
+  long st = (long)gridDim.x*blockDim.x;
+  for (; i < n; i += st) p[i] = 0;
+}
 __global__ void k_fused(const float* __restrict__ tf, const float* __restrict__ st,
                         const float* __restrict__ fg, const float* __restrict__ fbe,
                         const float* __restrict__ feat, float* __restrict__ fused){
@@ -648,47 +665,57 @@
   v = fmaxf((v - st[c*2])*st[c*2+1]*fg[c] + fbe[c], 0.f);
   fused[idx] = v + feat[idx];
 }
-__global__ void k_table(const int* __restrict__ ind, int* __restrict__ table){
-  int p = blockIdx.x*blockDim.x + threadIdx.x;
-  if (p >= NPTS) return;
-  int b = ind[p*4], z = ind[p*4+1], y = ind[p*4+2], x = ind[p*4+3];
-  table[((b*32+z)*32+y)*32+x] = p;
-}
-__global__ void k_nbr(const int* __restrict__ ind, const int* __restrict__ table,
-                      int* __restrict__ nbrtab){
+__global__ void k_bnrelu(const float* __restrict__ a, const float* __restrict__ st,
+                         const float* __restrict__ g, const float* __restrict__ be,
+                         float* __restrict__ o){
   int idx = blockIdx.x*blockDim.x + threadIdx.x;
-  if (idx >= NPTS*27) return;
-  int p = idx/27, tap = idx - p*27;
-  int dz = tap/9 - 1;
-  int rm = tap % 9;
-  int dy = rm/3 - 1, dx = rm%3 - 1;
-  int b = ind[p*4], z = ind[p*4+1]+dz, y = ind[p*4+2]+dy, x = ind[p*4+3]+dx;
-  int q = -1;
-  if ((unsigned)z < 32u && (unsigned)y < 32u && (unsigned)x < 32u)
-    q = table[((b*32+z)*32+y)*32+x];
-  nbrtab[idx] = q;
-}
-__global__ void __launch_bounds__(256) k_convlist(const int* __restrict__ nbrtab,
-                                                  int* __restrict__ tapcnt,
-                                                  int* __restrict__ ptlist){
+  int c = idx % CH;
+  float v = a[idx];
+  o[idx] = fmaxf((v - st[c*2])*st[c*2+1]*g[c] + be[c], 0.f);
+}
+
+__global__ void __launch_bounds__(256) k_nbrlist(const int* __restrict__ ind,
+                                                 const int* __restrict__ table,
+                                                 int* __restrict__ nbrtab,
+                                                 int* __restrict__ tapcnt,
+                                                 int* __restrict__ ptlist){
+  __shared__ int pb[256], pz[256], py[256], px[256];
   __shared__ int lcnt[27], lbase[27], lpos[27];
   int tid = threadIdx.x;
   if (tid < 27){ lcnt[tid] = 0; lpos[tid] = 0; }
-  __syncthreads();
-  int base = blockIdx.x * 6912;
-  for (int i = tid; i < 6912; i += 256){
-    int idx = base + i;
-    if (nbrtab[idx] >= 0) atomicAdd(&lcnt[idx % 27], 1);
+  int p0 = blockIdx.x*256;
+  pb[tid] = ind[(p0+tid)*4];
+  pz[tid] = ind[(p0+tid)*4+1];
+  py[tid] = ind[(p0+tid)*4+2];
+  px[tid] = ind[(p0+tid)*4+3];
+  __syncthreads();
+  int base = blockIdx.x*6912;
+  int qv[27];
+  #pragma unroll 1
+  for (int j = 0; j < 27; ++j){
+    int i = tid + j*256;
+    int pl = i/27, tap = i - pl*27;
+    int dz = tap/9 - 1;
+    int rm = tap % 9;
+    int dy = rm/3 - 1, dx = rm%3 - 1;
+    int z = pz[pl]+dz, y = py[pl]+dy, x = px[pl]+dx;
+    int q = -1;
+    if ((unsigned)z < 32u && (unsigned)y < 32u && (unsigned)x < 32u)
+      q = table[((pb[pl]*32+z)*32+y)*32+x];
+    qv[j] = q;
+    nbrtab[base + i] = q;
+    if (q >= 0) atomicAdd(&lcnt[tap], 1);
   }
   __syncthreads();
   if (tid < 27) lbase[tid] = atomicAdd(&tapcnt[tid], lcnt[tid]);
   __syncthreads();
-  for (int i = tid; i < 6912; i += 256){
-    int idx = base + i;
-    int q = nbrtab[idx];
+  #pragma unroll 1
+  for (int j = 0; j < 27; ++j){
+    int q = qv[j];
     if (q >= 0){
-      int tap = idx % 27;
-      int p = idx / 27;
+      int i = tid + j*256;
+      int tap = i % 27;
+      int p = p0 + i/27;
       int pos = lbase[tap] + atomicAdd(&lpos[tap], 1);
       ptlist[tap*NPTS + pos] = (p<<16) | q;
     }
@@ -697,7 +724,9 @@
 __global__ void __launch_bounds__(256) k_conv_gemm(
     const float* __restrict__ src, const float* __restrict__ Wc,
     const int* __restrict__ tapcnt, const int* __restrict__ ptlist,
-    float* __restrict__ part){
+    const float* __restrict__ bnst, const float* __restrict__ bng,
+    const float* __restrict__ bnbe, const float* __restrict__ res,
+    int fmode, float* __restrict__ part){
   int tap = blockIdx.y;
   int n = tapcnt[tap];
   int r0 = blockIdx.x*32;
@@ -720,16 +749,28 @@
   for (int idx4 = tid; idx4 < 32*24; idx4 += 256){
     int ir = idx4/24, c4 = idx4 - ir*24;
     int pq = pqs[ir];
-    float4 s = make_float4(0.f,0.f,0.f,0.f);
+    float4 s4 = make_float4(0.f,0.f,0.f,0.f);
     if (pq >= 0){
       int q = pq & 0xFFFF;
-      s = ((const float4*)(src + (long)q*CH))[c4];
+      s4 = ((const float4*)(src + (long)q*CH))[c4];
+      if (fmode){
+        int c0 = c4*4;
+        float vx = fmaxf((s4.x - bnst[(c0+0)*2])*bnst[(c0+0)*2+1]*bng[c0+0] + bnbe[c0+0], 0.f);
+        float vy = fmaxf((s4.y - bnst[(c0+1)*2])*bnst[(c0+1)*2+1]*bng[c0+1] + bnbe[c0+1], 0.f);
+        float vz = fmaxf((s4.z - bnst[(c0+2)*2])*bnst[(c0+2)*2+1]*bng[c0+2] + bnbe[c0+2], 0.f);
+        float vw = fmaxf((s4.w - bnst[(c0+3)*2])*bnst[(c0+3)*2+1]*bng[c0+3] + bnbe[c0+3], 0.f);
+        if (fmode == 2){
+          const float* rr = res + (long)q*CH + c0;
+          vx += rr[0]; vy += rr[1]; vz += rr[2]; vw += rr[3];
+        }
+        s4 = make_float4(vx,vy,vz,vw);
+      }
     }
     int k0 = c4*4;
-    Alt[(k0+0)*34 + ir] = s.x;
-    Alt[(k0+1)*34 + ir] = s.y;
-    Alt[(k0+2)*34 + ir] = s.z;
-    Alt[(k0+3)*34 + ir] = s.w;
+    Alt[(k0+0)*34 + ir] = s4.x;
+    Alt[(k0+1)*34 + ir] = s4.y;
+    Alt[(k0+2)*34 + ir] = s4.z;
+    Alt[(k0+3)*34 + ir] = s4.w;
   }
   __syncthreads();
   int rp = tid >> 4, cg = tid & 15;
@@ -748,14 +789,14 @@
     acc0[4] = fmaf(a.x, w2.x, acc0[4]); acc1[4] = fmaf(a.y, w2.x, acc1[4]);
     acc0[5] = fmaf(a.x, w2.y, acc0[5]); acc1[5] = fmaf(a.y, w2.y, acc1[5]);
   }
-  int pa = pqs[ra], pb = pqs[rb];
+  int pa = pqs[ra], pb2 = pqs[rb];
   if (pa >= 0){
     float* o = part + ((long)(pa>>16)*27 + tap)*CH + co0;
     #pragma unroll
     for (int j=0;j<6;++j) o[j] = acc0[j];
   }
-  if (pb >= 0){
-    float* o = part + ((long)(pb>>16)*27 + tap)*CH + co0;
+  if (pb2 >= 0){
+    float* o = part + ((long)(pb2>>16)*27 + tap)*CH + co0;
     #pragma unroll
     for (int j=0;j<6;++j) o[j] = acc1[j];
   }
@@ -835,22 +876,16 @@
     for (int j=0;j<6;++j) atomicAdd(&o[j], acc1[j]);
   }
 }
-__global__ void k_bnrelu(const float* __restrict__ a, const float* __restrict__ st,
-                         const float* __restrict__ g, const float* __restrict__ be,
-                         float* __restrict__ o){
+__global__ void k_final(const float* __restrict__ c2, const float* __restrict__ st12,
+                        const float* __restrict__ g2, const float* __restrict__ be2,
+                        const float* __restrict__ tf, const float* __restrict__ st10,
+                        const float* __restrict__ fg, const float* __restrict__ fbe,
+                        const float* __restrict__ feat, float* __restrict__ out){
   int idx = blockIdx.x*blockDim.x + threadIdx.x;
   int c = idx % CH;
-  float v = a[idx];
-  o[idx] = fmaxf((v - st[c*2])*st[c*2+1]*g[c] + be[c], 0.f);
-}
-__global__ void k_final(const float* __restrict__ c2, const float* __restrict__ st,
-                        const float* __restrict__ g, const float* __restrict__ be,
-                        const float* __restrict__ fused, float* __restrict__ out){
-  int idx = blockIdx.x*blockDim.x + threadIdx.x;
-  int c = idx % CH;
-  float v = c2[idx];
-  v = (v - st[c*2])*st[c*2+1]*g[c] + be[c];
-  out[idx] = fmaxf(v + fused[idx], 0.f);
+  float fsd = fmaxf((tf[idx] - st10[c*2])*st10[c*2+1]*fg[c] + fbe[c], 0.f) + feat[idx];
+  float v = (c2[idx] - st12[c*2])*st12[c*2+1]*g2[c] + be2[c];
+  out[idx] = fmaxf(v + fsd, 0.f);
 }
 
 extern "C" void kernel_launch(void* const* d_in, const int* in_sizes, int n_in,
@@ -911,7 +946,7 @@
   };
   const size_t FNC = (size_t)NCELEM*4;
   size_t o_packed = alloc((size_t)NPTS*4);
-  size_t o_start  = alloc(16);
+  size_t o_start  = alloc(32);
   size_t o_ball   = alloc((size_t)NBALL*4);
   size_t o_dens   = alloc((size_t)NPTS*4);
   size_t o_lin    = alloc((size_t)NPTS*4);
@@ -921,10 +956,8 @@
   size_t o_gsz    = alloc((size_t)NPTS*3*4);
   size_t o_reps   = alloc(16*4);
   size_t o_bkt    = alloc((size_t)3*100*3*4);
-  size_t o_cbuf   = alloc((size_t)3*NPTS*3*4);
   size_t o_ids    = alloc((size_t)3*NPTS*8);
   size_t o_seg    = alloc((size_t)3*NPTS*4);
-  size_t o_adp    = alloc((size_t)NPTS*3*4);
   size_t o_table  = alloc((size_t)65536*4);
   size_t o_nbr    = alloc((size_t)NPTS*27*4);
   size_t o_ptlist = alloc((size_t)27*NPTS*4);
@@ -938,7 +971,7 @@
   size_t o_cnt    = alloc((size_t)3*NPTS*4);
   size_t o_rank   = alloc((size_t)NPTS*4);
   size_t o_tapcnt = alloc(32*4);
-  size_t o_mx     = alloc(16*4);
+  size_t o_done   = alloc(16);
   size_t o_maxenc = alloc(16*4);
   size_t zend = off;
   size_t o_T96 = alloc(FNC);
@@ -959,12 +992,10 @@
   float* stats = (float*)(ws + o_stats);
   long zcount = (long)((zend - o_S)/4);
 
-  k_zero<<<dim3(2048), dim3(256), 0, stream>>>((int*)(ws+o_S), zcount);
-  k_init<<<dim3(256), dim3(256), 0, stream>>>((int*)(ws+o_table), (int*)(ws+o_start));
-  k_htinit<<<dim3((3*HTSZ+255)/256), dim3(256), 0, stream>>>((unsigned long long*)(ws+o_htk), (int*)(ws+o_htv));
-  k_pack_min<<<dim3(24), dim3(256), 0, stream>>>(ind, (unsigned*)(ws+o_packed), (int*)(ws+o_start));
-  k_table<<<dim3(24), 256, 0, stream>>>(ind, (int*)(ws+o_table));
-  k_ball<<<dim3(1), 256, 0, stream>>>((unsigned*)(ws+o_ball));
+  k_setup0<<<dim3(2048), dim3(256), 0, stream>>>((int*)(ws+o_S), zcount,
+      (unsigned long long*)(ws+o_htk), (int*)(ws+o_htv), (int*)(ws+o_table), (int*)(ws+o_start));
+  k_setup1<<<dim3(25), 256, 0, stream>>>(ind, (unsigned*)(ws+o_packed),
+      (int*)(ws+o_start), (int*)(ws+o_table), (unsigned*)(ws+o_ball));
 
   k_mm<<<dim3(192,1), 256, 0, stream>>>(x, fp_w, fp_b, (float*)(ws+o_t9), 96, 9,
       0,0,0,0, nullptr,0, nullptr,nullptr,0, nullptr,nullptr,nullptr, nullptr, 0);
@@ -991,12 +1022,10 @@
       (float*)(ws+o_dens), (float*)(ws+o_lin), (float*)(ws+o_gsz), (float*)(ws+o_gm));
 
   k_rank<<<dim3(24,8), 256, 0, stream>>>((float*)(ws+o_gm), (int*)(ws+o_rank));
-  k_scatter<<<dim3(24), 256, 0, stream>>>((int*)(ws+o_rank), (float*)(ws+o_gsz), (float*)(ws+o_bkt));
-  k_reps<<<dim3(1), 64, 0, stream>>>((float*)(ws+o_bkt), (float*)(ws+o_reps));
-
-  k_cluster_c<<<dim3(24,3), 256, 0, stream>>>(ind, (float*)(ws+o_reps), (int*)(ws+o_start),
-      (int*)(ws+o_cbuf), (int*)(ws+o_mx));
-  k_cluster_ids<<<dim3(24,3), 256, 0, stream>>>(ind, (int*)(ws+o_cbuf), (int*)(ws+o_mx),
+  k_scatter_reps<<<dim3(24), 256, 0, stream>>>((int*)(ws+o_rank), (float*)(ws+o_gsz),
+      (float*)(ws+o_bkt), (int*)(ws+o_done), (float*)(ws+o_reps));
+
+  k_cluster<<<dim3(24,3), 256, 0, stream>>>(ind, (float*)(ws+o_reps), (int*)(ws+o_start),
       (long long*)(ws+o_ids));
   k_seg_build<<<dim3(24,3), 256, 0, stream>>>((long long*)(ws+o_ids),
       (unsigned long long*)(ws+o_htk), (int*)(ws+o_htv));
@@ -1018,42 +1047,41 @@
   k_stats<<<dim3(96,4), 256, 0, stream>>>((float*)(ws+o_tp), NCELEM, 96, stats+6*192, 192);
   k_pf_accum<<<dim3(2304,3), 256, 0, stream>>>((float*)(ws+o_tp), stats+6*192, proj_g, proj_be,
       (float*)(ws+o_pw2), (unsigned*)(ws+o_maxenc), (int*)(ws+o_seg), (float*)(ws+o_E), (float*)(ws+o_F));
-  k_adp<<<dim3(24), 256, 0, stream>>>((float*)(ws+o_feat), adp_w, (float*)(ws+o_adp));
-  k_agg<<<dim3(2304), 256, 0, stream>>>((float*)(ws+o_adp), (float*)(ws+o_F), (int*)(ws+o_seg),
-      (float*)(ws+o_agg));
+  k_adp_agg<<<dim3(192), 256, 0, stream>>>((float*)(ws+o_feat), adp_w, (float*)(ws+o_F),
+      (int*)(ws+o_seg), (float*)(ws+o_agg));
 
   k_mm_fuse<<<dim3(192), 256, 0, stream>>>((float*)(ws+o_tp) + (size_t)3*NCELEM, stats+9*192,
       proj_g + 3*96, proj_be + 3*96, (float*)(ws+o_agg), fuse_w, (float*)(ws+o_tf));
   k_stats<<<dim3(96,1), 256, 0, stream>>>((float*)(ws+o_tf), 0, 96, stats+10*192, 0);
-  k_fused<<<dim3(2304), 256, 0, stream>>>((float*)(ws+o_tf), stats+10*192, fuse_g, fuse_be,
-      (float*)(ws+o_feat), (float*)(ws+o_fsd));
-
-  k_nbr<<<dim3((NPTS*27+255)/256), 256, 0, stream>>>(ind, (int*)(ws+o_table), (int*)(ws+o_nbr));
-  k_convlist<<<dim3(24), 256, 0, stream>>>((int*)(ws+o_nbr), (int*)(ws+o_tapcnt),
-      (int*)(ws+o_ptlist));
+
+  k_nbrlist<<<dim3(24), 256, 0, stream>>>(ind, (int*)(ws+o_table), (int*)(ws+o_nbr),
+      (int*)(ws+o_tapcnt), (int*)(ws+o_ptlist));
   if (use_part){
-    k_conv_gemm<<<dim3(192,27), 256, 0, stream>>>((float*)(ws+o_fsd), conv1_w,
-        (int*)(ws+o_tapcnt), (int*)(ws+o_ptlist), (float*)(ws+o_part));
+    k_conv_gemm<<<dim3(192,27), 256, 0, stream>>>((float*)(ws+o_tf), conv1_w,
+        (int*)(ws+o_tapcnt), (int*)(ws+o_ptlist),
+        stats+10*192, fuse_g, fuse_be, (float*)(ws+o_feat), 2, (float*)(ws+o_part));
     k_conv_sum<<<dim3(NPTS*24/256), 256, 0, stream>>>((int*)(ws+o_nbr), (float*)(ws+o_part),
         (float*)(ws+o_c1));
+    k_stats<<<dim3(96,1), 256, 0, stream>>>((float*)(ws+o_c1), 0, 96, stats+11*192, 0);
+    k_conv_gemm<<<dim3(192,27), 256, 0, stream>>>((float*)(ws+o_c1), conv2_w,
+        (int*)(ws+o_tapcnt), (int*)(ws+o_ptlist),
+        stats+11*192, bn1_g, bn1_be, nullptr, 1, (float*)(ws+o_part));
+    k_conv_sum<<<dim3(NPTS*24/256), 256, 0, stream>>>((int*)(ws+o_nbr), (float*)(ws+o_part),
+        (float*)(ws+o_c2));
   } else {
+    k_fused<<<dim3(2304), 256, 0, stream>>>((float*)(ws+o_tf), stats+10*192, fuse_g, fuse_be,
+        (float*)(ws+o_feat), (float*)(ws+o_fsd));
     k_zero<<<dim3(2304), dim3(256), 0, stream>>>((int*)(ws+o_c1), NCELEM);
     k_conv_gemm_atomic<<<dim3(192,27), 256, 0, stream>>>((float*)(ws+o_fsd), conv1_w,
         (int*)(ws+o_tapcnt), (int*)(ws+o_ptlist), (float*)(ws+o_c1));
-  }
-  k_stats<<<dim3(96,1), 256, 0, stream>>>((float*)(ws+o_c1), 0, 96, stats+11*192, 0);
-  k_bnrelu<<<dim3(2304), 256, 0, stream>>>((float*)(ws+o_c1), stats+11*192, bn1_g, bn1_be, (float*)(ws+o_f1));
-  if (use_part){
-    k_conv_gemm<<<dim3(192,27), 256, 0, stream>>>((float*)(ws+o_f1), conv2_w,
-        (int*)(ws+o_tapcnt), (int*)(ws+o_ptlist), (float*)(ws+o_part));
-    k_conv_sum<<<dim3(NPTS*24/256), 256, 0, stream>>>((int*)(ws+o_nbr), (float*)(ws+o_part),
-        (float*)(ws+o_c2));
-  } else {
+    k_stats<<<dim3(96,1), 256, 0, stream>>>((float*)(ws+o_c1), 0, 96, stats+11*192, 0);
+    k_bnrelu<<<dim3(2304), 256, 0, stream>>>((float*)(ws+o_c1), stats+11*192, bn1_g, bn1_be,
+        (float*)(ws+o_f1));
     k_zero<<<dim3(2304), dim3(256), 0, stream>>>((int*)(ws+o_c2), NCELEM);
     k_conv_gemm_atomic<<<dim3(192,27), 256, 0, stream>>>((float*)(ws+o_f1), conv2_w,
         (int*)(ws+o_tapcnt), (int*)(ws+o_ptlist), (float*)(ws+o_c2));
   }
   k_stats<<<dim3(96,1), 256, 0, stream>>>((float*)(ws+o_c2), 0, 96, stats+12*192, 0);
   k_final<<<dim3(2304), 256, 0, stream>>>((float*)(ws+o_c2), stats+12*192, bn2_g, bn2_be,
-      (float*)(ws+o_fsd), outp);
-}
+      (float*)(ws+o_tf), stats+10*192, fuse_g, fuse_be, (float*)(ws+o_feat), outp);
+}
```

New measurement: 486.6 us, median of 2. 1.03x faster.
